# Optimization experiments

Hardware: AMD Instinct MI355X
Metric: run time of the kernel (lower is better)

The kernel has to match this reference:

```python
import jax, jax.numpy as jnp
import numpy as np

C = 1.0
SQC = C ** 0.5
EPS = 1e-15

def _artanh(x):
    return jnp.arctanh(jnp.clip(x, -1 + 1e-5, 1 - 1e-5))

def _norm(x):
    return jnp.sqrt(jnp.maximum(jnp.sum(x * x, -1, keepdims=True), EPS))

def expmap0(u):
    un = _norm(u)
    return jnp.tanh(SQC * un) * u / (SQC * un)

def logmap0(x):
    xn = _norm(x)
    return _artanh(SQC * xn) * x / (SQC * xn)

def project(x):
    maxnorm = (1.0 - 1e-3) / SQC
    xn = _norm(x)
    return jnp.where(xn > maxnorm, x / xn * maxnorm, x)

def mobius_add(x, y):
    x2 = jnp.sum(x * x, -1, keepdims=True)
    y2 = jnp.sum(y * y, -1, keepdims=True)
    xy = jnp.sum(x * y, -1, keepdims=True)
    num = (1 + 2 * C * xy + C * y2) * x + (1 - C * x2) * y
    den = 1 + 2 * C * xy + C * C * x2 * y2
    return num / jnp.maximum(den, EPS)

def mobius_matvec(M, x):
    xn = _norm(x)
    Mx = x @ M.T
    Mxn = _norm(Mx)
    res = jnp.tanh(Mxn / xn * _artanh(SQC * xn)) * Mx / (Mxn * SQC)
    return jnp.where(Mxn <= 1e-7, jnp.zeros_like(res), res)

def mobius_pointwise_mul(w, x):
    xn = _norm(x)
    wx = w * x
    wxn = _norm(wx)
    res = jnp.tanh(wxn / xn * _artanh(SQC * xn)) * wx / (wxn * SQC)
    return jnp.where(wxn <= 1e-7, jnp.zeros_like(res), res)

def mobius_scalar_mul(r, x):
    # r: [B,1] scalars, x: [P] point -> [B,P]
    xn = _norm(x)
    return jnp.tanh(r * _artanh(SQC * xn)) * x / (xn * SQC)

def poincare_dist(x, y):
    return 2.0 / SQC * _artanh(SQC * _norm(mobius_add(-x, y)))

def dist2plane(x, p, a):
    # x: [B,P], p,a: [K,P] -> [B,K]
    diff = mobius_add(-p[None, :, :], x[:, None, :])  # [B,K,P]
    diff2 = jnp.sum(diff * diff, -1)
    sc_da = jnp.sum(diff * a[None, :, :], -1)
    a_norm = jnp.sqrt(jnp.maximum(jnp.sum(a * a, -1), EPS))  # [K]
    num = 2 * SQC * sc_da
    den = jnp.maximum((1 - C * diff2) * a_norm[None, :], EPS)
    return jnp.arcsinh(num / den) / SQC

def one_rnn_transform(W, h, U, x, b):
    Wh = mobius_matvec(W, h)
    Ux = mobius_matvec(U, x)
    return mobius_add(mobius_add(Wh, Ux), b)

def mobius_gru(x_seq, w_ih, w_hh, b, h0):
    # x_seq: [S,B,E]; w_ih: [3,H,E]; w_hh: [3,H,H]; b: [3,H]
    W_ir, W_ih_, W_iz = w_ih[0], w_ih[1], w_ih[2]
    W_hr, W_hh_, W_hz = w_hh[0], w_hh[1], w_hh[2]
    b_r, b_h, b_z = b[0], b[1], b[2]

    def cell(h, x):
        z = jax.nn.sigmoid(logmap0(one_rnn_transform(W_hz, h, W_iz, x, b_z)))
        r = jax.nn.sigmoid(logmap0(one_rnn_transform(W_hr, h, W_ir, x, b_r)))
        rh = mobius_pointwise_mul(r, h)
        h_tilde = one_rnn_transform(W_hh_, rh, W_ih_, x, b_h)
        delta = mobius_add(-h, h_tilde)
        h_new = mobius_add(h, mobius_pointwise_mul(z, delta))
        return h_new, None

    h_final, _ = jax.lax.scan(cell, h0, x_seq)
    return h_final

def mobius_linear(x, W, b):
    return project(mobius_add(mobius_matvec(W, x), b))


def setup_inputs() -> dict:
    key = jax.random.key(0)
    ks = jax.random.split(key, 20)
    V, E, H, P, K, B, S = 32000, 256, 512, 256, 2, 512, 100
    inp = {
        "embedding": jax.random.normal(ks[0], (V, E), jnp.float32) * 0.1,
        "w_ih_src": jax.random.normal(ks[1], (3, H, E), jnp.float32) * 0.05,
        "w_hh_src": jax.random.normal(ks[2], (3, H, H), jnp.float32) * 0.05,
        "b_src": jax.random.normal(ks[3], (3, H), jnp.float32) * 0.01,
        "w_ih_tgt": jax.random.normal(ks[4], (3, H, E), jnp.float32) * 0.05,
        "w_hh_tgt": jax.random.normal(ks[5], (3, H, H), jnp.float32) * 0.05,
        "b_tgt": jax.random.normal(ks[6], (3, H), jnp.float32) * 0.01,
        "wp_src": jax.random.normal(ks[7], (P, H), jnp.float32) * 0.05,
        "bp_src": jax.random.normal(ks[8], (P,), jnp.float32) * 0.01,
        "wp_tgt": jax.random.normal(ks[9], (P, H), jnp.float32) * 0.05,
        "bp_tgt": jax.random.normal(ks[10], (P,), jnp.float32) * 0.01,
        "dist_bias": jax.random.normal(ks[11], (P,), jnp.float32) * 0.01,
        "plane_p": jax.random.normal(ks[12], (K, P), jnp.float32) * 0.01,
        "plane_a": jax.random.normal(ks[13], (K, P), jnp.float32) * 0.1,
        "source_tokens": jax.random.randint(ks[14], (B, S), 0, V, jnp.int32),
        "target_tokens": jax.random.randint(ks[15], (B, S), 0, V, jnp.int32),
        "alignment": jax.random.randint(ks[16], (B,), 0, B, jnp.int32),
    }
    return inp


def reference(embedding, w_ih_src, w_hh_src, b_src, w_ih_tgt, w_hh_tgt, b_tgt,
              wp_src, bp_src, wp_tgt, bp_tgt, dist_bias, plane_p, plane_a,
              source_tokens, target_tokens, alignment):
    B, S = source_tokens.shape
    H = w_hh_src.shape[-1]
    # euclidean embeddings lifted to the Poincare ball (embedding_type='eucl', hyp cell)
    src = expmap0(embedding[source_tokens]).transpose(1, 0, 2)  # [S,B,E]
    tgt = expmap0(embedding[target_tokens]).transpose(1, 0, 2)
    h0 = jnp.zeros((B, H), src.dtype)
    h_src = mobius_gru(src, w_ih_src, w_hh_src, b_src, h0)
    h_tgt = mobius_gru(tgt, w_ih_tgt, w_hh_tgt, b_tgt, h0)
    h_tgt = h_tgt[alignment]
    src_proj = mobius_linear(h_src, wp_src, bp_src)
    tgt_proj = mobius_linear(h_tgt, wp_tgt, bp_tgt)
    projected = mobius_add(src_proj, tgt_proj)
    d2 = poincare_dist(h_src, h_tgt) ** 2  # [B,1]
    bias = mobius_scalar_mul(d2, dist_bias)  # [B,P]
    projected = mobius_add(projected, bias)
    logits = dist2plane(projected, plane_p, plane_a)  # [B,K]
    return logits
```

## Files before the change

kernel.cpp:

```cpp
#include <hip/hip_runtime.h>
#include <hip/hip_bf16.h>

#define EPSF 1e-15f

__device__ __forceinline__ float artanh_c(float x) {
  x = fminf(fmaxf(x, -1.f + 1e-5f), 1.f - 1e-5f);
  return 0.5f * log1pf(2.f * x / (1.f - x));
}
__device__ __forceinline__ float sigmoidf(float x) {
  return 1.f / (1.f + expf(-x));
}

template<int N>
__device__ __forceinline__ void block_reduce(float* v) {
  __shared__ float s[4][N];
  __syncthreads();
  const int lane = threadIdx.x & 63;
  const int wv = threadIdx.x >> 6;
#pragma unroll
  for (int n = 0; n < N; n++) {
    float x = v[n];
#pragma unroll
    for (int o = 32; o > 0; o >>= 1) x += __shfl_down(x, o);
    if (lane == 0) s[wv][n] = x;
  }
  __syncthreads();
#pragma unroll
  for (int n = 0; n < N; n++) v[n] = s[0][n] + s[1][n] + s[2][n] + s[3][n];
}

__global__ __launch_bounds__(256) void k_tok(
    const float* __restrict__ emb, const int* __restrict__ src_t,
    const int* __restrict__ tgt_t, float4* __restrict__ tokf)
{
  const int item = blockIdx.x * 4 + (threadIdx.x >> 6);
  const int lane = threadIdx.x & 63;
  const int g = item / 51200;
  const int rem = item - g * 51200;
  const int b = rem / 100, s = rem - b * 100;
  const int tok = (g ? tgt_t : src_t)[b * 100 + s];
  const float4 v = ((const float4*)(emb + (size_t)tok * 256))[lane];
  float ss = v.x*v.x + v.y*v.y + v.z*v.z + v.w*v.w;
#pragma unroll
  for (int o = 32; o > 0; o >>= 1) ss += __shfl_xor(ss, o);
  if (lane == 0) {
    const float un = sqrtf(fmaxf(ss, EPSF));
    const float fac = tanhf(un) / un;
    const float xn = sqrtf(fmaxf(fac * fac * ss, EPSF));
    const float axn = artanh_c(xn);
    tokf[item] = make_float4(fac, xn, axn, un);
  }
}

__global__ __launch_bounds__(256) void kx0(
    const float* __restrict__ emb, const int* __restrict__ src_t,
    const int* __restrict__ tgt_t, const float4* __restrict__ tokf,
    float* __restrict__ xb)
{
  const int row = blockIdx.x;
  const int t = threadIdx.x;
  const int g = row >> 9, b = row & 511;
  const int tok = (g ? tgt_t : src_t)[b * 100];
  const float fac = tokf[(g * 512 + b) * 100].x;
  xb[(size_t)row * 256 + t] = fac * emb[(size_t)tok * 256 + t];
}

__global__ __launch_bounds__(256) void gemm_k(
    int mode,
    const float* __restrict__ hbuf, const float* __restrict__ xbuf,
    const float* __restrict__ rhbuf,
    const float* __restrict__ w_ih_src, const float* __restrict__ w_hh_src,
    const float* __restrict__ w_ih_tgt, const float* __restrict__ w_hh_tgt,
    const float* __restrict__ wp_src, const float* __restrict__ wp_tgt,
    const int* __restrict__ alignment,
    float* __restrict__ out)
{
  const int rt = blockIdx.x, ct = blockIdx.y;
  const int rowBase = rt * 64;
  const int tid = threadIdx.x;
  int kdim, ldo, colBase;
  const float* W;
  const float* Abase;
  int gather = 0;
  if (mode == 0) {
    const int chunk = ct >> 3;
    colBase = ct * 64; ldo = 2560;
    const int g = rowBase >> 9;
    const float* wih = g ? w_ih_tgt : w_ih_src;
    const float* whh = g ? w_hh_tgt : w_hh_src;
    if (chunk == 0)      { W = whh + 2 * 512 * 512; Abase = hbuf; kdim = 512; }
    else if (chunk == 1) { W = whh;                 Abase = hbuf; kdim = 512; }
    else {
      kdim = 256; Abase = xbuf;
      W = (chunk == 2) ? (wih + 2 * 512 * 256) : ((chunk == 3) ? wih : (wih + 512 * 256));
    }
    W += (size_t)((ct & 7) * 64) * kdim;
  } else if (mode == 1) {
    const int g = rowBase >> 9;
    W = (g ? w_hh_tgt : w_hh_src) + 512 * 512 + (size_t)(ct * 64) * 512;
    Abase = rhbuf; kdim = 512; ldo = 512; colBase = ct * 64;
  } else {
    const int chunk = ct >> 2;
    colBase = ct * 64; ldo = 512; kdim = 512;
    W = (chunk ? wp_tgt : wp_src) + (size_t)((ct & 3) * 64) * 512;
    Abase = hbuf;
    gather = chunk;
  }
  const int ar = tid >> 2, ak = (tid & 3) * 4;
  int arow = rowBase + ar;
  if (mode == 2 && gather) arow = 512 + alignment[arow];
  const float* Arow = Abase + (size_t)arow * kdim;
  const float* Wrow = W + (size_t)(tid >> 2) * kdim + (tid & 3) * 4;

  __shared__ __align__(16) float As[16][68];
  __shared__ __align__(16) float Bs[16][68];
  float acc[4][4] = {{0.f}};
  const int ty = tid >> 4, tx = tid & 15;

  for (int k0 = 0; k0 < kdim; k0 += 16) {
    const float4 av = *(const float4*)(Arow + k0 + ak);
    const float4 bv = *(const float4*)(Wrow + k0);
    const int bj = tid >> 2;
    As[ak + 0][ar] = av.x; As[ak + 1][ar] = av.y; As[ak + 2][ar] = av.z; As[ak + 3][ar] = av.w;
    Bs[ak + 0][bj] = bv.x; Bs[ak + 1][bj] = bv.y; Bs[ak + 2][bj] = bv.z; Bs[ak + 3][bj] = bv.w;
    __syncthreads();
#pragma unroll
    for (int kk = 0; kk < 16; kk++) {
      const float4 a4 = *(const float4*)(&As[kk][ty * 4]);
      const float4 b4 = *(const float4*)(&Bs[kk][tx * 4]);
      acc[0][0] += a4.x * b4.x; acc[0][1] += a4.x * b4.y; acc[0][2] += a4.x * b4.z; acc[0][3] += a4.x * b4.w;
      acc[1][0] += a4.y * b4.x; acc[1][1] += a4.y * b4.y; acc[1][2] += a4.y * b4.z; acc[1][3] += a4.y * b4.w;
      acc[2][0] += a4.z * b4.x; acc[2][1] += a4.z * b4.y; acc[2][2] += a4.z * b4.z; acc[2][3] += a4.z * b4.w;
      acc[3][0] += a4.w * b4.x; acc[3][1] += a4.w * b4.y; acc[3][2] += a4.w * b4.z; acc[3][3] += a4.w * b4.w;
    }
    __syncthreads();
  }
#pragma unroll
  for (int r = 0; r < 4; r++) {
    float4 o; o.x = acc[r][0]; o.y = acc[r][1]; o.z = acc[r][2]; o.w = acc[r][3];
    *(float4*)(out + (size_t)(rowBase + ty * 4 + r) * ldo + colBase + tx * 4) = o;
  }
}

__global__ __launch_bounds__(256) void k2_gates(
    const float* __restrict__ g1, const float* __restrict__ hb,
    const float* __restrict__ b_src, const float* __restrict__ b_tgt,
    const float4* __restrict__ tokf,
    float* __restrict__ zb, float* __restrict__ rhb,
    float* __restrict__ uhxb, float* __restrict__ rn, int s)
{
  const int row = blockIdx.x;
  const int g = row >> 9, b = row & 511;
  const int t = threadIdx.x;
  const float* bb = g ? b_tgt : b_src;
  const float4 tf = tokf[(g * 512 + b) * 100 + s];
  const float xn_x = tf.y, axn_x = tf.z;
  const float* grow = g1 + (size_t)row * 2560;
  const float* hrow = hb + (size_t)row * 512;

  float h[2], whz[2], whr[2], uxz[2], uxr[2], uxh[2], bz[2], br[2];
  float r6[6] = {0, 0, 0, 0, 0, 0};
#pragma unroll
  for (int e = 0; e < 2; e++) {
    const int j = t + e * 256;
    h[e] = hrow[j];
    whz[e] = grow[j];        whr[e] = grow[512 + j];
    uxz[e] = grow[1024 + j]; uxr[e] = grow[1536 + j];
    uxh[e] = grow[2048 + j];
    bz[e] = bb[1024 + j];    br[e] = bb[j];
    r6[0] += h[e] * h[e];     r6[1] += whz[e] * whz[e]; r6[2] += whr[e] * whr[e];
    r6[3] += uxz[e] * uxz[e]; r6[4] += uxr[e] * uxr[e]; r6[5] += uxh[e] * uxh[e];
  }
  block_reduce<6>(r6);
  const float sh2 = r6[0];
  const float xn_h = sqrtf(fmaxf(sh2, EPSF)), axn_h = artanh_c(xn_h);

  const float mz = sqrtf(fmaxf(r6[1], EPSF)); const float tz = tanhf(mz / xn_h * axn_h);
  const float sz = (mz <= 1e-7f) ? 0.f : tz / mz; const float x2z = (mz <= 1e-7f) ? 0.f : tz * tz;
  const float mr = sqrtf(fmaxf(r6[2], EPSF)); const float tr = tanhf(mr / xn_h * axn_h);
  const float sr = (mr <= 1e-7f) ? 0.f : tr / mr; const float x2r = (mr <= 1e-7f) ? 0.f : tr * tr;
  const float muz = sqrtf(fmaxf(r6[3], EPSF)); const float tuz = tanhf(muz / xn_x * axn_x);
  const float suz = (muz <= 1e-7f) ? 0.f : tuz / muz; const float y2z = (muz <= 1e-7f) ? 0.f : tuz * tuz;
  const float mur = sqrtf(fmaxf(r6[4], EPSF)); const float tur = tanhf(mur / xn_x * axn_x);
  const float sur = (mur <= 1e-7f) ? 0.f : tur / mur; const float y2r = (mur <= 1e-7f) ? 0.f : tur * tur;
  const float muh = sqrtf(fmaxf(r6[5], EPSF)); const float tuh = tanhf(muh / xn_x * axn_x);
  const float suh = (muh <= 1e-7f) ? 0.f : tuh / muh; const float y2u = (muh <= 1e-7f) ? 0.f : tuh * tuh;

  float Wz[2], Uz[2], Wr[2], Ur[2];
  float dd[2] = {0, 0};
#pragma unroll
  for (int e = 0; e < 2; e++) {
    Wz[e] = sz * whz[e]; Uz[e] = suz * uxz[e];
    Wr[e] = sr * whr[e]; Ur[e] = sur * uxr[e];
    dd[0] += Wz[e] * Uz[e]; dd[1] += Wr[e] * Ur[e];
  }
  block_reduce<2>(dd);
  float t1z[2], t1r[2];
  {
    const float xy = dd[0];
    const float iv = 1.f / fmaxf(1.f + 2.f * xy + x2z * y2z, EPSF);
    const float c1 = 1.f + 2.f * xy + y2z, c2 = 1.f - x2z;
#pragma unroll
    for (int e = 0; e < 2; e++) t1z[e] = (c1 * Wz[e] + c2 * Uz[e]) * iv;
  }
  {
    const float xy = dd[1];
    const float iv = 1.f / fmaxf(1.f + 2.f * xy + x2r * y2r, EPSF);
    const float c1 = 1.f + 2.f * xy + y2r, c2 = 1.f - x2r;
#pragma unroll
    for (int e = 0; e < 2; e++) t1r[e] = (c1 * Wr[e] + c2 * Ur[e]) * iv;
  }
  float r6b[6] = {0, 0, 0, 0, 0, 0};
#pragma unroll
  for (int e = 0; e < 2; e++) {
    r6b[0] += t1z[e] * t1z[e]; r6b[1] += t1z[e] * bz[e]; r6b[2] += bz[e] * bz[e];
    r6b[3] += t1r[e] * t1r[e]; r6b[4] += t1r[e] * br[e]; r6b[5] += br[e] * br[e];
  }
  block_reduce<6>(r6b);
  float t2z[2], t2r[2];
  {
    const float x2 = r6b[0], xy = r6b[1], y2 = r6b[2];
    const float iv = 1.f / fmaxf(1.f + 2.f * xy + x2 * y2, EPSF);
    const float c1 = 1.f + 2.f * xy + y2, c2 = 1.f - x2;
#pragma unroll
    for (int e = 0; e < 2; e++) t2z[e] = (c1 * t1z[e] + c2 * bz[e]) * iv;
  }
  {
    const float x2 = r6b[3], xy = r6b[4], y2 = r6b[5];
    const float iv = 1.f / fmaxf(1.f + 2.f * xy + x2 * y2, EPSF);
    const float c1 = 1.f + 2.f * xy + y2, c2 = 1.f - x2;
#pragma unroll
    for (int e = 0; e < 2; e++) t2r[e] = (c1 * t1r[e] + c2 * br[e]) * iv;
  }
  float nn[2] = {0, 0};
#pragma unroll
  for (int e = 0; e < 2; e++) { nn[0] += t2z[e] * t2z[e]; nn[1] += t2r[e] * t2r[e]; }
  block_reduce<2>(nn);
  const float nz = sqrtf(fmaxf(nn[0], EPSF)); const float fz = artanh_c(nz) / nz;
  const float nr = sqrtf(fmaxf(nn[1], EPSF)); const float fr = artanh_c(nr) / nr;
  float zz[2], wx[2];
  float rw[1] = {0};
#pragma unroll
  for (int e = 0; e < 2; e++) {
    zz[e] = sigmoidf(fz * t2z[e]);
    const float rr = sigmoidf(fr * t2r[e]);
    wx[e] = rr * h[e];
    rw[0] += wx[e] * wx[e];
  }
  block_reduce<1>(rw);
  const float wxn = sqrtf(fmaxf(rw[0], EPSF));
  const float trh = tanhf(wxn / xn_h * axn_h);
  const float srh = (wxn <= 1e-7f) ? 0.f : trh / wxn;
  const float xn_rh = (wxn <= 1e-7f) ? sqrtf(EPSF) : fmaxf(trh, sqrtf(EPSF));
  const float axn_rh = artanh_c(xn_rh);
#pragma unroll
  for (int e = 0; e < 2; e++) {
    const int j = t + e * 256;
    zb[(size_t)row * 512 + j] = zz[e];
    rhb[(size_t)row * 512 + j] = srh * wx[e];
    uhxb[(size_t)row * 512 + j] = suh * uxh[e];
  }
  if (t == 0) {
    float* r8 = rn + row * 8;
    r8[0] = xn_h; r8[1] = axn_h; r8[2] = xn_rh; r8[3] = axn_rh; r8[4] = y2u; r8[5] = sh2;
  }
}

__global__ __launch_bounds__(256) void k4_update(
    const float* __restrict__ htm, const float* __restrict__ uhxb,
    const float* __restrict__ zb, float* __restrict__ hb,
    const float* __restrict__ b_src, const float* __restrict__ b_tgt,
    const float* __restrict__ rn, const float4* __restrict__ tokf,
    const int* __restrict__ src_t, const int* __restrict__ tgt_t,
    const float* __restrict__ emb, float* __restrict__ xb, int s)
{
  const int row = blockIdx.x;
  const int g = row >> 9, b = row & 511;
  const int t = threadIdx.x;
  const float* bb = g ? b_tgt : b_src;
  const float* r8 = rn + row * 8;
  const float xn_rh = r8[2], axn_rh = r8[3], y2u = r8[4], sh2 = r8[5];

  float mt_[2], ux[2], z[2], h[2], bh[2];
  float rA[2] = {0, 0};
#pragma unroll
  for (int e = 0; e < 2; e++) {
    const int j = t + e * 256;
    mt_[e] = htm[(size_t)row * 512 + j];
    ux[e] = uhxb[(size_t)row * 512 + j];
    z[e] = zb[(size_t)row * 512 + j];
    h[e] = hb[(size_t)row * 512 + j];
    bh[e] = bb[512 + j];
    rA[0] += mt_[e] * mt_[e];
    rA[1] += mt_[e] * ux[e];
  }
  block_reduce<2>(rA);
  const float m = sqrtf(fmaxf(rA[0], EPSF));
  const float tt = tanhf(m / xn_rh * axn_rh);
  const float st = (m <= 1e-7f) ? 0.f : tt / m;
  const float x2 = (m <= 1e-7f) ? 0.f : tt * tt;
  float t1[2];
  {
    const float xy = st * rA[1];
    const float iv = 1.f / fmaxf(1.f + 2.f * xy + x2 * y2u, EPSF);
    const float c1 = 1.f + 2.f * xy + y2u, c2 = 1.f - x2;
#pragma unroll
    for (int e = 0; e < 2; e++) t1[e] = (c1 * (st * mt_[e]) + c2 * ux[e]) * iv;
  }
  float rB[3] = {0, 0, 0};
#pragma unroll
  for (int e = 0; e < 2; e++) {
    rB[0] += t1[e] * t1[e]; rB[1] += t1[e] * bh[e]; rB[2] += bh[e] * bh[e];
  }
  block_reduce<3>(rB);
  float ht[2];
  {
    const float x2b = rB[0], xy = rB[1], y2 = rB[2];
    const float iv = 1.f / fmaxf(1.f + 2.f * xy + x2b * y2, EPSF);
    const float c1 = 1.f + 2.f * xy + y2, c2 = 1.f - x2b;
#pragma unroll
    for (int e = 0; e < 2; e++) ht[e] = (c1 * t1[e] + c2 * bh[e]) * iv;
  }
  float rC[2] = {0, 0};
#pragma unroll
  for (int e = 0; e < 2; e++) { rC[0] += ht[e] * ht[e]; rC[1] += h[e] * ht[e]; }
  block_reduce<2>(rC);
  float delta[2];
  {
    const float y2 = rC[0], xy = -rC[1];
    const float iv = 1.f / fmaxf(1.f + 2.f * xy + sh2 * y2, EPSF);
    const float c1 = 1.f + 2.f * xy + y2, c2 = 1.f - sh2;
#pragma unroll
    for (int e = 0; e < 2; e++) delta[e] = (c1 * (-h[e]) + c2 * ht[e]) * iv;
  }
  float rD[3] = {0, 0, 0};
#pragma unroll
  for (int e = 0; e < 2; e++) {
    const float w = z[e] * delta[e];
    rD[0] += delta[e] * delta[e];
    rD[1] += w * w;
    rD[2] += h[e] * w;
  }
  block_reduce<3>(rD);
  const float dn = sqrtf(fmaxf(rD[0], EPSF));
  const float axnd = artanh_c(dn);
  const float wxn = sqrtf(fmaxf(rD[1], EPSF));
  const float tzd = tanhf(wxn / dn * axnd);
  const float szd = (wxn <= 1e-7f) ? 0.f : tzd / wxn;
  const float y2zd = (wxn <= 1e-7f) ? 0.f : tzd * tzd;
  {
    const float xy = szd * rD[2];
    const float iv = 1.f / fmaxf(1.f + 2.f * xy + sh2 * y2zd, EPSF);
    const float c1 = 1.f + 2.f * xy + y2zd, c2 = 1.f - sh2;
#pragma unroll
    for (int e = 0; e < 2; e++) {
      const int j = t + e * 256;
      hb[(size_t)row * 512 + j] = (c1 * h[e] + c2 * (szd * z[e] * delta[e])) * iv;
    }
  }
  if (s + 1 < 100) {
    const int tok = (g ? tgt_t : src_t)[b * 100 + s + 1];
    const float fac = tokf[(g * 512 + b) * 100 + s + 1].x;
    xb[(size_t)row * 256 + t] = fac * emb[(size_t)tok * 256 + t];
  }
}

__global__ __launch_bounds__(256) void k_head(
    const float* __restrict__ hb, const float* __restrict__ mxb,
    const float* __restrict__ bp_src, const float* __restrict__ bp_tgt,
    const float* __restrict__ dist_bias, const float* __restrict__ plane_p,
    const float* __restrict__ plane_a, const int* __restrict__ alignment,
    float* __restrict__ outp)
{
  const int b = blockIdx.x;
  const int t = threadIdx.x;
  const int arow = 512 + alignment[b];
  float hs[2], htg[2];
  hs[0] = hb[(size_t)b * 512 + t];      hs[1] = hb[(size_t)b * 512 + 256 + t];
  htg[0] = hb[(size_t)arow * 512 + t];  htg[1] = hb[(size_t)arow * 512 + 256 + t];
  const float mxs = mxb[(size_t)b * 512 + t];
  const float mxt = mxb[(size_t)b * 512 + 256 + t];
  const float bps = bp_src[t], bpt = bp_tgt[t], db = dist_bias[t];
  const float pp0 = plane_p[t], pp1 = plane_p[256 + t];
  const float pa0 = plane_a[t], pa1 = plane_a[256 + t];

  float rA[5] = {0, 0, 0, 0, 0};
#pragma unroll
  for (int e = 0; e < 2; e++) {
    rA[0] += hs[e] * hs[e]; rA[1] += htg[e] * htg[e]; rA[2] += hs[e] * htg[e];
  }
  rA[3] = mxs * mxs; rA[4] = mxt * mxt;
  block_reduce<5>(rA);
  const float shs = rA[0], sht = rA[1], dot_st = rA[2];
  const float xns = sqrtf(fmaxf(shs, EPSF)), axns = artanh_c(xns);
  const float xnt = sqrtf(fmaxf(sht, EPSF)), axnt = artanh_c(xnt);
  const float ms = sqrtf(fmaxf(rA[3], EPSF)); const float ts = tanhf(ms / xns * axns);
  const float ss = (ms <= 1e-7f) ? 0.f : ts / ms; const float x2s = (ms <= 1e-7f) ? 0.f : ts * ts;
  const float mt = sqrtf(fmaxf(rA[4], EPSF)); const float tt = tanhf(mt / xnt * axnt);
  const float st = (mt <= 1e-7f) ? 0.f : tt / mt; const float x2t = (mt <= 1e-7f) ? 0.f : tt * tt;
  const float vs = ss * mxs, vt = st * mxt;

  float rB[5] = {bps * bps, vs * bps, bpt * bpt, vt * bpt, db * db};
  block_reduce<5>(rB);
  float ps, pt;
  {
    const float y2 = rB[0], xy = rB[1];
    const float iv = 1.f / fmaxf(1.f + 2.f * xy + x2s * y2, EPSF);
    ps = ((1.f + 2.f * xy + y2) * vs + (1.f - x2s) * bps) * iv;
  }
  {
    const float y2 = rB[2], xy = rB[3];
    const float iv = 1.f / fmaxf(1.f + 2.f * xy + x2t * y2, EPSF);
    pt = ((1.f + 2.f * xy + y2) * vt + (1.f - x2t) * bpt) * iv;
  }
  float rC[2] = {ps * ps, pt * pt};
  block_reduce<2>(rC);
  {
    const float n = sqrtf(fmaxf(rC[0], EPSF));
    if (n > 0.999f) ps *= 0.999f / n;
  }
  {
    const float n = sqrtf(fmaxf(rC[1], EPSF));
    if (n > 0.999f) pt *= 0.999f / n;
  }
  float df[2];
  {
    const float xy = -dot_st;
    const float iv = 1.f / fmaxf(1.f + 2.f * xy + shs * sht, EPSF);
    const float c1 = 1.f + 2.f * xy + sht, c2 = 1.f - shs;
#pragma unroll
    for (int e = 0; e < 2; e++) df[e] = (c1 * (-hs[e]) + c2 * htg[e]) * iv;
  }
  float rD[4] = {ps * ps, pt * pt, ps * pt, df[0] * df[0] + df[1] * df[1]};
  block_reduce<4>(rD);
  float pr;
  {
    const float x2 = rD[0], y2 = rD[1], xy = rD[2];
    const float iv = 1.f / fmaxf(1.f + 2.f * xy + x2 * y2, EPSF);
    pr = ((1.f + 2.f * xy + y2) * ps + (1.f - x2) * pt) * iv;
  }
  const float dn = sqrtf(fmaxf(rD[3], EPSF));
  const float dist = 2.f * artanh_c(dn);
  const float d2v = dist * dist;
  const float dbn = sqrtf(fmaxf(rB[4], EPSF));
  const float biasv = tanhf(d2v * artanh_c(dbn)) * db / dbn;

  float rE[3] = {pr * pr, biasv * biasv, pr * biasv};
  block_reduce<3>(rE);
  float pr2;
  {
    const float x2 = rE[0], y2 = rE[1], xy = rE[2];
    const float iv = 1.f / fmaxf(1.f + 2.f * xy + x2 * y2, EPSF);
    pr2 = ((1.f + 2.f * xy + y2) * pr + (1.f - x2) * biasv) * iv;
  }
  float rF[5] = {pp0 * pp0, pp0 * pr2, pp1 * pp1, pp1 * pr2, pr2 * pr2};
  block_reduce<5>(rF);
  float d0, d1;
  {
    const float x2 = rF[0], xy = -rF[1], y2 = rF[4];
    const float iv = 1.f / fmaxf(1.f + 2.f * xy + x2 * y2, EPSF);
    d0 = ((1.f + 2.f * xy + y2) * (-pp0) + (1.f - x2) * pr2) * iv;
  }
  {
    const float x2 = rF[2], xy = -rF[3], y2 = rF[4];
    const float iv = 1.f / fmaxf(1.f + 2.f * xy + x2 * y2, EPSF);
    d1 = ((1.f + 2.f * xy + y2) * (-pp1) + (1.f - x2) * pr2) * iv;
  }
  float rG[6] = {d0 * d0, d0 * pa0, pa0 * pa0, d1 * d1, d1 * pa1, pa1 * pa1};
  block_reduce<6>(rG);
  if (t == 0) {
    const float an0 = sqrtf(fmaxf(rG[2], EPSF));
    const float an1 = sqrtf(fmaxf(rG[5], EPSF));
    const float l0 = asinhf(2.f * rG[1] / fmaxf((1.f - rG[0]) * an0, EPSF));
    const float l1 = asinhf(2.f * rG[4] / fmaxf((1.f - rG[3]) * an1, EPSF));
    outp[b * 2 + 0] = l0;
    outp[b * 2 + 1] = l1;
  }
}

extern "C" void kernel_launch(void* const* d_in, const int* in_sizes, int n_in,
                              void* d_out, int out_size, void* d_ws, size_t ws_size,
                              hipStream_t stream) {
  const float* emb       = (const float*)d_in[0];
  const float* w_ih_src  = (const float*)d_in[1];
  const float* w_hh_src  = (const float*)d_in[2];
  const float* b_src     = (const float*)d_in[3];
  const float* w_ih_tgt  = (const float*)d_in[4];
  const float* w_hh_tgt  = (const float*)d_in[5];
  const float* b_tgt     = (const float*)d_in[6];
  const float* wp_src    = (const float*)d_in[7];
  const float* bp_src    = (const float*)d_in[8];
  const float* wp_tgt    = (const float*)d_in[9];
  const float* bp_tgt    = (const float*)d_in[10];
  const float* dist_bias = (const float*)d_in[11];
  const float* plane_p   = (const float*)d_in[12];
  const float* plane_a   = (const float*)d_in[13];
  const int* src_t       = (const int*)d_in[14];
  const int* tgt_t       = (const int*)d_in[15];
  const int* alignment   = (const int*)d_in[16];
  float* outp            = (float*)d_out;

  float* ws = (float*)d_ws;
  float* hbuf = ws + 0;
  float* xbuf = ws + 524288;
  float* g1   = ws + 786432;
  float* zb   = ws + 3407872;
  float* rhb  = ws + 3932160;
  float* uhxb = ws + 4456448;
  float* htm  = ws + 4980736;
  float* rn   = ws + 5505024;
  float4* tokf = (float4*)(ws + 5513216);
  float* mxb  = ws + 5922816;

  hipMemsetAsync(hbuf, 0, 1024 * 512 * sizeof(float), stream);
  k_tok<<<25600, 256, 0, stream>>>(emb, src_t, tgt_t, tokf);
  kx0<<<1024, 256, 0, stream>>>(emb, src_t, tgt_t, tokf, xbuf);
  for (int s = 0; s < 100; s++) {
    gemm_k<<<dim3(16, 40), 256, 0, stream>>>(0, hbuf, xbuf, rhb,
        w_ih_src, w_hh_src, w_ih_tgt, w_hh_tgt, wp_src, wp_tgt, alignment, g1);
    k2_gates<<<1024, 256, 0, stream>>>(g1, hbuf, b_src, b_tgt, tokf, zb, rhb, uhxb, rn, s);
    gemm_k<<<dim3(16, 8), 256, 0, stream>>>(1, hbuf, xbuf, rhb,
        w_ih_src, w_hh_src, w_ih_tgt, w_hh_tgt, wp_src, wp_tgt, alignment, htm);
    k4_update<<<1024, 256, 0, stream>>>(htm, uhxb, zb, hbuf, b_src, b_tgt, rn, tokf,
        src_t, tgt_t, emb, xbuf, s);
  }
  gemm_k<<<dim3(8, 8), 256, 0, stream>>>(2, hbuf, xbuf, rhb,
      w_ih_src, w_hh_src, w_ih_tgt, w_hh_tgt, wp_src, wp_tgt, alignment, mxb);
  k_head<<<512, 256, 0, stream>>>(hbuf, mxb, bp_src, bp_tgt, dist_bias,
      plane_p, plane_a, alignment, outp);
}
```

Before: 8.037 ms.

## Replace per-step kernel launches with cooperative persistent kernel using split-bf16 MFMA

Replaces the 400 per-timestep launches (two FP32 SIMT GEMMs plus gate and update kernels) with one cooperative persistent kernel that uses grid syncs between phases. The GEMMs now run on MFMA bf16 instructions with a hi/lo split (three products) to approximate FP32 accuracy, using weights pre-split by a new conversion kernel. Row reductions move from block-level shared-memory reductions to wave-level shuffles. This removes launch overhead and scalar FMA cost, but relies on grid-wide barriers and accepts slightly lower precision from dropping the lo*lo term.

```diff
diff --git a/kernel.cpp b/kernel.cpp
--- a/kernel.cpp
+++ b/kernel.cpp
@@ -1,32 +1,71 @@
 #include <hip/hip_runtime.h>
 #include <hip/hip_bf16.h>
+#include <hip/hip_cooperative_groups.h>
+
+namespace cg = cooperative_groups;
 
 #define EPSF 1e-15f
+
+typedef __hip_bfloat16 bf16;
+typedef __attribute__((ext_vector_type(8))) short short8;
+typedef __attribute__((ext_vector_type(4))) float f32x4;
+
+#define F4E(v,i) ((i)==0?(v).x:((i)==1?(v).y:((i)==2?(v).z:(v).w)))
+#define U4E(v,i) ((i)==0?(v).x:((i)==1?(v).y:((i)==2?(v).z:(v).w)))
 
 __device__ __forceinline__ float artanh_c(float x) {
   x = fminf(fmaxf(x, -1.f + 1e-5f), 1.f - 1e-5f);
   return 0.5f * log1pf(2.f * x / (1.f - x));
 }
-__device__ __forceinline__ float sigmoidf(float x) {
-  return 1.f / (1.f + expf(-x));
-}
-
-template<int N>
-__device__ __forceinline__ void block_reduce(float* v) {
-  __shared__ float s[4][N];
-  __syncthreads();
-  const int lane = threadIdx.x & 63;
-  const int wv = threadIdx.x >> 6;
-#pragma unroll
-  for (int n = 0; n < N; n++) {
-    float x = v[n];
-#pragma unroll
-    for (int o = 32; o > 0; o >>= 1) x += __shfl_down(x, o);
-    if (lane == 0) s[wv][n] = x;
-  }
-  __syncthreads();
-#pragma unroll
-  for (int n = 0; n < N; n++) v[n] = s[0][n] + s[1][n] + s[2][n] + s[3][n];
+__device__ __forceinline__ float sigmoidf(float x) { return 1.f / (1.f + expf(-x)); }
+__device__ __forceinline__ float wave_sum(float x) {
+#pragma unroll
+  for (int o = 32; o > 0; o >>= 1) x += __shfl_xor(x, o);
+  return x;
+}
+__device__ __forceinline__ float bu2f(ushort u) { return __uint_as_float(((unsigned)u) << 16); }
+__device__ __forceinline__ ushort f2bu(float v) {
+  bf16 t = __float2bfloat16(v);
+  union { bf16 b; ushort u; } c; c.b = t; return c.u;
+}
+__device__ __forceinline__ void split2(float v, ushort& h, ushort& l) {
+  h = f2bu(v); l = f2bu(v - bu2f(h));
+}
+
+__global__ __launch_bounds__(256) void k_wconv(
+    const float* __restrict__ w_ih_src, const float* __restrict__ w_hh_src,
+    const float* __restrict__ w_ih_tgt, const float* __restrict__ w_hh_tgt,
+    const float* __restrict__ wp_src, const float* __restrict__ wp_tgt,
+    bf16* __restrict__ W0h, bf16* __restrict__ W0l,
+    bf16* __restrict__ W1h, bf16* __restrict__ W1l,
+    bf16* __restrict__ W2h, bf16* __restrict__ W2l)
+{
+  const int idx = blockIdx.x * 256 + threadIdx.x;
+  float v; bf16 *ph, *pl; int oi;
+  if (idx < 1835008) {
+    const int g = idx / 917504, r = idx % 917504;
+    const float* wih = g ? w_ih_tgt : w_ih_src;
+    const float* whh = g ? w_hh_tgt : w_hh_src;
+    if (r < 262144)      v = whh[524288 + r];
+    else if (r < 524288) v = whh[r - 262144];
+    else if (r < 655360) v = wih[262144 + (r - 524288)];
+    else if (r < 786432) v = wih[r - 655360];
+    else                 v = wih[131072 + (r - 786432)];
+    ph = W0h; pl = W0l; oi = idx;
+  } else if (idx < 2359296) {
+    const int j = idx - 1835008;
+    const int g = j >> 18, r = j & 262143;
+    v = (g ? w_hh_tgt : w_hh_src)[262144 + r];
+    ph = W1h; pl = W1l; oi = j;
+  } else {
+    const int p = idx - 2359296;
+    if (p >= 262144) return;
+    const int g = p >> 17, r = p & 131071;
+    v = (g ? wp_tgt : wp_src)[r];
+    ph = W2h; pl = W2l; oi = p;
+  }
+  ushort hh, ll; split2(v, hh, ll);
+  ((ushort*)ph)[oi] = hh; ((ushort*)pl)[oi] = ll;
 }
 
 __global__ __launch_bounds__(256) void k_tok(
@@ -47,434 +86,579 @@
     const float un = sqrtf(fmaxf(ss, EPSF));
     const float fac = tanhf(un) / un;
     const float xn = sqrtf(fmaxf(fac * fac * ss, EPSF));
-    const float axn = artanh_c(xn);
-    tokf[item] = make_float4(fac, xn, axn, un);
+    tokf[item] = make_float4(fac, xn, artanh_c(xn), un);
   }
 }
 
 __global__ __launch_bounds__(256) void kx0(
     const float* __restrict__ emb, const int* __restrict__ src_t,
     const int* __restrict__ tgt_t, const float4* __restrict__ tokf,
-    float* __restrict__ xb)
+    bf16* __restrict__ Xh, bf16* __restrict__ Xl)
 {
   const int row = blockIdx.x;
   const int t = threadIdx.x;
   const int g = row >> 9, b = row & 511;
   const int tok = (g ? tgt_t : src_t)[b * 100];
   const float fac = tokf[(g * 512 + b) * 100].x;
-  xb[(size_t)row * 256 + t] = fac * emb[(size_t)tok * 256 + t];
-}
-
-__global__ __launch_bounds__(256) void gemm_k(
-    int mode,
-    const float* __restrict__ hbuf, const float* __restrict__ xbuf,
-    const float* __restrict__ rhbuf,
-    const float* __restrict__ w_ih_src, const float* __restrict__ w_hh_src,
-    const float* __restrict__ w_ih_tgt, const float* __restrict__ w_hh_tgt,
-    const float* __restrict__ wp_src, const float* __restrict__ wp_tgt,
-    const int* __restrict__ alignment,
-    float* __restrict__ out)
+  ushort hh, ll; split2(fac * emb[(size_t)tok * 256 + t], hh, ll);
+  ((ushort*)Xh)[(size_t)row * 256 + t] = hh;
+  ((ushort*)Xl)[(size_t)row * 256 + t] = ll;
+}
+
+__device__ __forceinline__ void mma_32x32(
+    const bf16* __restrict__ Ah, const bf16* __restrict__ Al,
+    size_t a0, size_t a1,
+    const bf16* __restrict__ Wh, const bf16* __restrict__ Wl,
+    size_t b0, size_t b1, int K,
+    float* __restrict__ outB, int ldo, int kg)
 {
-  const int rt = blockIdx.x, ct = blockIdx.y;
-  const int rowBase = rt * 64;
+  f32x4 acc00 = {0,0,0,0}, acc01 = {0,0,0,0}, acc10 = {0,0,0,0}, acc11 = {0,0,0,0};
+#pragma unroll 2
+  for (int k0 = 0; k0 < K; k0 += 32) {
+    const short8 a0h = *(const short8*)(Ah + a0 + k0);
+    const short8 a0l = *(const short8*)(Al + a0 + k0);
+    const short8 a1h = *(const short8*)(Ah + a1 + k0);
+    const short8 a1l = *(const short8*)(Al + a1 + k0);
+    const short8 b0h = *(const short8*)(Wh + b0 + k0);
+    const short8 b0l = *(const short8*)(Wl + b0 + k0);
+    const short8 b1h = *(const short8*)(Wh + b1 + k0);
+    const short8 b1l = *(const short8*)(Wl + b1 + k0);
+    acc00 = __builtin_amdgcn_mfma_f32_16x16x32_bf16(a0h, b0h, acc00, 0, 0, 0);
+    acc01 = __builtin_amdgcn_mfma_f32_16x16x32_bf16(a0h, b1h, acc01, 0, 0, 0);
+    acc10 = __builtin_amdgcn_mfma_f32_16x16x32_bf16(a1h, b0h, acc10, 0, 0, 0);
+    acc11 = __builtin_amdgcn_mfma_f32_16x16x32_bf16(a1h, b1h, acc11, 0, 0, 0);
+    acc00 = __builtin_amdgcn_mfma_f32_16x16x32_bf16(a0h, b0l, acc00, 0, 0, 0);
+    acc01 = __builtin_amdgcn_mfma_f32_16x16x32_bf16(a0h, b1l, acc01, 0, 0, 0);
+    acc10 = __builtin_amdgcn_mfma_f32_16x16x32_bf16(a1h, b0l, acc10, 0, 0, 0);
+    acc11 = __builtin_amdgcn_mfma_f32_16x16x32_bf16(a1h, b1l, acc11, 0, 0, 0);
+    acc00 = __builtin_amdgcn_mfma_f32_16x16x32_bf16(a0l, b0h, acc00, 0, 0, 0);
+    acc01 = __builtin_amdgcn_mfma_f32_16x16x32_bf16(a0l, b1h, acc01, 0, 0, 0);
+    acc10 = __builtin_amdgcn_mfma_f32_16x16x32_bf16(a1l, b0h, acc10, 0, 0, 0);
+    acc11 = __builtin_amdgcn_mfma_f32_16x16x32_bf16(a1l, b1h, acc11, 0, 0, 0);
+  }
+#pragma unroll
+  for (int r = 0; r < 4; r++) {
+    outB[(size_t)(kg*4 + r) * ldo]            = acc00[r];
+    outB[(size_t)(kg*4 + r) * ldo + 16]       = acc01[r];
+    outB[(size_t)(16 + kg*4 + r) * ldo]       = acc10[r];
+    outB[(size_t)(16 + kg*4 + r) * ldo + 16]  = acc11[r];
+  }
+}
+
+__device__ __forceinline__ void mma_32x16(
+    const bf16* __restrict__ Ah, const bf16* __restrict__ Al,
+    size_t a0, size_t a1,
+    const bf16* __restrict__ Wh, const bf16* __restrict__ Wl,
+    size_t b0, int K,
+    float* __restrict__ outB, int ldo, int kg)
+{
+  f32x4 acc0 = {0,0,0,0}, acc1 = {0,0,0,0};
+#pragma unroll 2
+  for (int k0 = 0; k0 < K; k0 += 32) {
+    const short8 a0h = *(const short8*)(Ah + a0 + k0);
+    const short8 a0l = *(const short8*)(Al + a0 + k0);
+    const short8 a1h = *(const short8*)(Ah + a1 + k0);
+    const short8 a1l = *(const short8*)(Al + a1 + k0);
+    const short8 bh  = *(const short8*)(Wh + b0 + k0);
+    const short8 bl  = *(const short8*)(Wl + b0 + k0);
+    acc0 = __builtin_amdgcn_mfma_f32_16x16x32_bf16(a0h, bh, acc0, 0, 0, 0);
+    acc1 = __builtin_amdgcn_mfma_f32_16x16x32_bf16(a1h, bh, acc1, 0, 0, 0);
+    acc0 = __builtin_amdgcn_mfma_f32_16x16x32_bf16(a0h, bl, acc0, 0, 0, 0);
+    acc1 = __builtin_amdgcn_mfma_f32_16x16x32_bf16(a1h, bl, acc1, 0, 0, 0);
+    acc0 = __builtin_amdgcn_mfma_f32_16x16x32_bf16(a0l, bh, acc0, 0, 0, 0);
+    acc1 = __builtin_amdgcn_mfma_f32_16x16x32_bf16(a1l, bh, acc1, 0, 0, 0);
+  }
+#pragma unroll
+  for (int r = 0; r < 4; r++) {
+    outB[(size_t)(kg*4 + r) * ldo]      = acc0[r];
+    outB[(size_t)(16 + kg*4 + r) * ldo] = acc1[r];
+  }
+}
+
+__device__ __forceinline__ void phaseA_tile(
+    int tr, int tc, int wr, int wc, int fr, int kg,
+    const bf16* Hh, const bf16* Hl, const bf16* Xh, const bf16* Xl,
+    const bf16* W0h, const bf16* W0l, float* g1)
+{
+  const int g = tr >> 9;
+  int K; const bf16 *Ah, *Al; size_t Woff;
+  if (tc < 1024) {
+    K = 512; Ah = Hh; Al = Hl;
+    Woff = (size_t)g*917504 + (size_t)(tc>>9)*262144 + (size_t)(tc & 511)*512;
+  } else {
+    K = 256; Ah = Xh; Al = Xl;
+    const int lc = tc - 1024;
+    Woff = (size_t)g*917504 + 524288 + (size_t)(lc>>9)*131072 + (size_t)(lc & 511)*256;
+  }
+  const int r0 = tr + wr*32;
+  const size_t a0 = (size_t)(r0 + fr)*K + kg*8, a1 = a0 + (size_t)16*K;
+  const size_t b0 = (size_t)(wc*32 + fr)*K + kg*8, b1 = b0 + (size_t)16*K;
+  float* outB = g1 + (size_t)r0*2560 + (tc + wc*32 + fr);
+  mma_32x32(Ah, Al, a0, a1, W0h + Woff, W0l + Woff, b0, b1, K, outB, 2560, kg);
+}
+
+struct CoopArgs {
+  const float *emb; const int *src_t, *tgt_t;
+  const float *b_src, *b_tgt, *bp_src, *bp_tgt, *dist_bias, *plane_p, *plane_a;
+  const int *alignment;
+  float *g1, *htm, *hbuf, *mxb;
+  const float4 *tokf;
+  bf16 *Hh, *Hl, *Xh, *Xl, *Rh, *Rl;
+  const bf16 *W0h, *W0l, *W1h, *W1l, *W2h, *W2l;
+  float *outp;
+};
+
+__global__ __launch_bounds__(512, 2) void k_coop(CoopArgs A)
+{
+  cg::grid_group grid = cg::this_grid();
+  const int bid = blockIdx.x;
   const int tid = threadIdx.x;
-  int kdim, ldo, colBase;
-  const float* W;
-  const float* Abase;
-  int gather = 0;
-  if (mode == 0) {
-    const int chunk = ct >> 3;
-    colBase = ct * 64; ldo = 2560;
-    const int g = rowBase >> 9;
-    const float* wih = g ? w_ih_tgt : w_ih_src;
-    const float* whh = g ? w_hh_tgt : w_hh_src;
-    if (chunk == 0)      { W = whh + 2 * 512 * 512; Abase = hbuf; kdim = 512; }
-    else if (chunk == 1) { W = whh;                 Abase = hbuf; kdim = 512; }
-    else {
-      kdim = 256; Abase = xbuf;
-      W = (chunk == 2) ? (wih + 2 * 512 * 256) : ((chunk == 3) ? wih : (wih + 512 * 256));
-    }
-    W += (size_t)((ct & 7) * 64) * kdim;
-  } else if (mode == 1) {
-    const int g = rowBase >> 9;
-    W = (g ? w_hh_tgt : w_hh_src) + 512 * 512 + (size_t)(ct * 64) * 512;
-    Abase = rhbuf; kdim = 512; ldo = 512; colBase = ct * 64;
+  const int w = tid >> 6, lane = tid & 63;
+  const int fr = lane & 15, kg = lane >> 4;
+  const int wrA = w >> 1, wcA = w & 1;
+  const int wrC = w >> 2, wcC = w & 3;
+
+  int An, t0r = 0, t0c = 0, t1r = 0, t1c = 0;
+  if (bid < 128) {
+    An = 1; t0r = (bid >> 4) * 128; t0c = (bid & 15) * 64;
   } else {
-    const int chunk = ct >> 2;
-    colBase = ct * 64; ldo = 512; kdim = 512;
-    W = (chunk ? wp_tgt : wp_src) + (size_t)((ct & 3) * 64) * 512;
-    Abase = hbuf;
-    gather = chunk;
-  }
-  const int ar = tid >> 2, ak = (tid & 3) * 4;
-  int arow = rowBase + ar;
-  if (mode == 2 && gather) arow = 512 + alignment[arow];
-  const float* Arow = Abase + (size_t)arow * kdim;
-  const float* Wrow = W + (size_t)(tid >> 2) * kdim + (tid & 3) * 4;
-
-  __shared__ __align__(16) float As[16][68];
-  __shared__ __align__(16) float Bs[16][68];
-  float acc[4][4] = {{0.f}};
-  const int ty = tid >> 4, tx = tid & 15;
-
-  for (int k0 = 0; k0 < kdim; k0 += 16) {
-    const float4 av = *(const float4*)(Arow + k0 + ak);
-    const float4 bv = *(const float4*)(Wrow + k0);
-    const int bj = tid >> 2;
-    As[ak + 0][ar] = av.x; As[ak + 1][ar] = av.y; As[ak + 2][ar] = av.z; As[ak + 3][ar] = av.w;
-    Bs[ak + 0][bj] = bv.x; Bs[ak + 1][bj] = bv.y; Bs[ak + 2][bj] = bv.z; Bs[ak + 3][bj] = bv.w;
-    __syncthreads();
-#pragma unroll
-    for (int kk = 0; kk < 16; kk++) {
-      const float4 a4 = *(const float4*)(&As[kk][ty * 4]);
-      const float4 b4 = *(const float4*)(&Bs[kk][tx * 4]);
-      acc[0][0] += a4.x * b4.x; acc[0][1] += a4.x * b4.y; acc[0][2] += a4.x * b4.z; acc[0][3] += a4.x * b4.w;
-      acc[1][0] += a4.y * b4.x; acc[1][1] += a4.y * b4.y; acc[1][2] += a4.y * b4.z; acc[1][3] += a4.y * b4.w;
-      acc[2][0] += a4.z * b4.x; acc[2][1] += a4.z * b4.y; acc[2][2] += a4.z * b4.z; acc[2][3] += a4.z * b4.w;
-      acc[3][0] += a4.w * b4.x; acc[3][1] += a4.w * b4.y; acc[3][2] += a4.w * b4.z; acc[3][3] += a4.w * b4.w;
-    }
-    __syncthreads();
-  }
-#pragma unroll
-  for (int r = 0; r < 4; r++) {
-    float4 o; o.x = acc[r][0]; o.y = acc[r][1]; o.z = acc[r][2]; o.w = acc[r][3];
-    *(float4*)(out + (size_t)(rowBase + ty * 4 + r) * ldo + colBase + tx * 4) = o;
-  }
-}
-
-__global__ __launch_bounds__(256) void k2_gates(
-    const float* __restrict__ g1, const float* __restrict__ hb,
-    const float* __restrict__ b_src, const float* __restrict__ b_tgt,
-    const float4* __restrict__ tokf,
-    float* __restrict__ zb, float* __restrict__ rhb,
-    float* __restrict__ uhxb, float* __restrict__ rn, int s)
-{
-  const int row = blockIdx.x;
-  const int g = row >> 9, b = row & 511;
-  const int t = threadIdx.x;
-  const float* bb = g ? b_tgt : b_src;
-  const float4 tf = tokf[(g * 512 + b) * 100 + s];
-  const float xn_x = tf.y, axn_x = tf.z;
-  const float* grow = g1 + (size_t)row * 2560;
-  const float* hrow = hb + (size_t)row * 512;
-
-  float h[2], whz[2], whr[2], uxz[2], uxr[2], uxh[2], bz[2], br[2];
-  float r6[6] = {0, 0, 0, 0, 0, 0};
-#pragma unroll
-  for (int e = 0; e < 2; e++) {
-    const int j = t + e * 256;
-    h[e] = hrow[j];
-    whz[e] = grow[j];        whr[e] = grow[512 + j];
-    uxz[e] = grow[1024 + j]; uxr[e] = grow[1536 + j];
-    uxh[e] = grow[2048 + j];
-    bz[e] = bb[1024 + j];    br[e] = bb[j];
-    r6[0] += h[e] * h[e];     r6[1] += whz[e] * whz[e]; r6[2] += whr[e] * whr[e];
-    r6[3] += uxz[e] * uxz[e]; r6[4] += uxr[e] * uxr[e]; r6[5] += uxh[e] * uxh[e];
-  }
-  block_reduce<6>(r6);
-  const float sh2 = r6[0];
-  const float xn_h = sqrtf(fmaxf(sh2, EPSF)), axn_h = artanh_c(xn_h);
-
-  const float mz = sqrtf(fmaxf(r6[1], EPSF)); const float tz = tanhf(mz / xn_h * axn_h);
-  const float sz = (mz <= 1e-7f) ? 0.f : tz / mz; const float x2z = (mz <= 1e-7f) ? 0.f : tz * tz;
-  const float mr = sqrtf(fmaxf(r6[2], EPSF)); const float tr = tanhf(mr / xn_h * axn_h);
-  const float sr = (mr <= 1e-7f) ? 0.f : tr / mr; const float x2r = (mr <= 1e-7f) ? 0.f : tr * tr;
-  const float muz = sqrtf(fmaxf(r6[3], EPSF)); const float tuz = tanhf(muz / xn_x * axn_x);
-  const float suz = (muz <= 1e-7f) ? 0.f : tuz / muz; const float y2z = (muz <= 1e-7f) ? 0.f : tuz * tuz;
-  const float mur = sqrtf(fmaxf(r6[4], EPSF)); const float tur = tanhf(mur / xn_x * axn_x);
-  const float sur = (mur <= 1e-7f) ? 0.f : tur / mur; const float y2r = (mur <= 1e-7f) ? 0.f : tur * tur;
-  const float muh = sqrtf(fmaxf(r6[5], EPSF)); const float tuh = tanhf(muh / xn_x * axn_x);
-  const float suh = (muh <= 1e-7f) ? 0.f : tuh / muh; const float y2u = (muh <= 1e-7f) ? 0.f : tuh * tuh;
-
-  float Wz[2], Uz[2], Wr[2], Ur[2];
-  float dd[2] = {0, 0};
-#pragma unroll
-  for (int e = 0; e < 2; e++) {
-    Wz[e] = sz * whz[e]; Uz[e] = suz * uxz[e];
-    Wr[e] = sr * whr[e]; Ur[e] = sur * uxr[e];
-    dd[0] += Wz[e] * Uz[e]; dd[1] += Wr[e] * Ur[e];
-  }
-  block_reduce<2>(dd);
-  float t1z[2], t1r[2];
-  {
-    const float xy = dd[0];
-    const float iv = 1.f / fmaxf(1.f + 2.f * xy + x2z * y2z, EPSF);
-    const float c1 = 1.f + 2.f * xy + y2z, c2 = 1.f - x2z;
-#pragma unroll
-    for (int e = 0; e < 2; e++) t1z[e] = (c1 * Wz[e] + c2 * Uz[e]) * iv;
-  }
-  {
-    const float xy = dd[1];
-    const float iv = 1.f / fmaxf(1.f + 2.f * xy + x2r * y2r, EPSF);
-    const float c1 = 1.f + 2.f * xy + y2r, c2 = 1.f - x2r;
-#pragma unroll
-    for (int e = 0; e < 2; e++) t1r[e] = (c1 * Wr[e] + c2 * Ur[e]) * iv;
-  }
-  float r6b[6] = {0, 0, 0, 0, 0, 0};
-#pragma unroll
-  for (int e = 0; e < 2; e++) {
-    r6b[0] += t1z[e] * t1z[e]; r6b[1] += t1z[e] * bz[e]; r6b[2] += bz[e] * bz[e];
-    r6b[3] += t1r[e] * t1r[e]; r6b[4] += t1r[e] * br[e]; r6b[5] += br[e] * br[e];
-  }
-  block_reduce<6>(r6b);
-  float t2z[2], t2r[2];
-  {
-    const float x2 = r6b[0], xy = r6b[1], y2 = r6b[2];
-    const float iv = 1.f / fmaxf(1.f + 2.f * xy + x2 * y2, EPSF);
-    const float c1 = 1.f + 2.f * xy + y2, c2 = 1.f - x2;
-#pragma unroll
-    for (int e = 0; e < 2; e++) t2z[e] = (c1 * t1z[e] + c2 * bz[e]) * iv;
-  }
-  {
-    const float x2 = r6b[3], xy = r6b[4], y2 = r6b[5];
-    const float iv = 1.f / fmaxf(1.f + 2.f * xy + x2 * y2, EPSF);
-    const float c1 = 1.f + 2.f * xy + y2, c2 = 1.f - x2;
-#pragma unroll
-    for (int e = 0; e < 2; e++) t2r[e] = (c1 * t1r[e] + c2 * br[e]) * iv;
-  }
-  float nn[2] = {0, 0};
-#pragma unroll
-  for (int e = 0; e < 2; e++) { nn[0] += t2z[e] * t2z[e]; nn[1] += t2r[e] * t2r[e]; }
-  block_reduce<2>(nn);
-  const float nz = sqrtf(fmaxf(nn[0], EPSF)); const float fz = artanh_c(nz) / nz;
-  const float nr = sqrtf(fmaxf(nn[1], EPSF)); const float fr = artanh_c(nr) / nr;
-  float zz[2], wx[2];
-  float rw[1] = {0};
-#pragma unroll
-  for (int e = 0; e < 2; e++) {
-    zz[e] = sigmoidf(fz * t2z[e]);
-    const float rr = sigmoidf(fr * t2r[e]);
-    wx[e] = rr * h[e];
-    rw[0] += wx[e] * wx[e];
-  }
-  block_reduce<1>(rw);
-  const float wxn = sqrtf(fmaxf(rw[0], EPSF));
-  const float trh = tanhf(wxn / xn_h * axn_h);
-  const float srh = (wxn <= 1e-7f) ? 0.f : trh / wxn;
-  const float xn_rh = (wxn <= 1e-7f) ? sqrtf(EPSF) : fmaxf(trh, sqrtf(EPSF));
-  const float axn_rh = artanh_c(xn_rh);
-#pragma unroll
-  for (int e = 0; e < 2; e++) {
-    const int j = t + e * 256;
-    zb[(size_t)row * 512 + j] = zz[e];
-    rhb[(size_t)row * 512 + j] = srh * wx[e];
-    uhxb[(size_t)row * 512 + j] = suh * uxh[e];
-  }
-  if (t == 0) {
-    float* r8 = rn + row * 8;
-    r8[0] = xn_h; r8[1] = axn_h; r8[2] = xn_rh; r8[3] = axn_rh; r8[4] = y2u; r8[5] = sh2;
-  }
-}
-
-__global__ __launch_bounds__(256) void k4_update(
-    const float* __restrict__ htm, const float* __restrict__ uhxb,
-    const float* __restrict__ zb, float* __restrict__ hb,
-    const float* __restrict__ b_src, const float* __restrict__ b_tgt,
-    const float* __restrict__ rn, const float4* __restrict__ tokf,
-    const int* __restrict__ src_t, const int* __restrict__ tgt_t,
-    const float* __restrict__ emb, float* __restrict__ xb, int s)
-{
-  const int row = blockIdx.x;
-  const int g = row >> 9, b = row & 511;
-  const int t = threadIdx.x;
-  const float* bb = g ? b_tgt : b_src;
-  const float* r8 = rn + row * 8;
-  const float xn_rh = r8[2], axn_rh = r8[3], y2u = r8[4], sh2 = r8[5];
-
-  float mt_[2], ux[2], z[2], h[2], bh[2];
-  float rA[2] = {0, 0};
-#pragma unroll
-  for (int e = 0; e < 2; e++) {
-    const int j = t + e * 256;
-    mt_[e] = htm[(size_t)row * 512 + j];
-    ux[e] = uhxb[(size_t)row * 512 + j];
-    z[e] = zb[(size_t)row * 512 + j];
-    h[e] = hb[(size_t)row * 512 + j];
-    bh[e] = bb[512 + j];
-    rA[0] += mt_[e] * mt_[e];
-    rA[1] += mt_[e] * ux[e];
-  }
-  block_reduce<2>(rA);
-  const float m = sqrtf(fmaxf(rA[0], EPSF));
-  const float tt = tanhf(m / xn_rh * axn_rh);
-  const float st = (m <= 1e-7f) ? 0.f : tt / m;
-  const float x2 = (m <= 1e-7f) ? 0.f : tt * tt;
-  float t1[2];
-  {
-    const float xy = st * rA[1];
-    const float iv = 1.f / fmaxf(1.f + 2.f * xy + x2 * y2u, EPSF);
-    const float c1 = 1.f + 2.f * xy + y2u, c2 = 1.f - x2;
-#pragma unroll
-    for (int e = 0; e < 2; e++) t1[e] = (c1 * (st * mt_[e]) + c2 * ux[e]) * iv;
-  }
-  float rB[3] = {0, 0, 0};
-#pragma unroll
-  for (int e = 0; e < 2; e++) {
-    rB[0] += t1[e] * t1[e]; rB[1] += t1[e] * bh[e]; rB[2] += bh[e] * bh[e];
-  }
-  block_reduce<3>(rB);
-  float ht[2];
-  {
-    const float x2b = rB[0], xy = rB[1], y2 = rB[2];
-    const float iv = 1.f / fmaxf(1.f + 2.f * xy + x2b * y2, EPSF);
-    const float c1 = 1.f + 2.f * xy + y2, c2 = 1.f - x2b;
-#pragma unroll
-    for (int e = 0; e < 2; e++) ht[e] = (c1 * t1[e] + c2 * bh[e]) * iv;
-  }
-  float rC[2] = {0, 0};
-#pragma unroll
-  for (int e = 0; e < 2; e++) { rC[0] += ht[e] * ht[e]; rC[1] += h[e] * ht[e]; }
-  block_reduce<2>(rC);
-  float delta[2];
-  {
-    const float y2 = rC[0], xy = -rC[1];
-    const float iv = 1.f / fmaxf(1.f + 2.f * xy + sh2 * y2, EPSF);
-    const float c1 = 1.f + 2.f * xy + y2, c2 = 1.f - sh2;
-#pragma unroll
-    for (int e = 0; e < 2; e++) delta[e] = (c1 * (-h[e]) + c2 * ht[e]) * iv;
-  }
-  float rD[3] = {0, 0, 0};
-#pragma unroll
-  for (int e = 0; e < 2; e++) {
-    const float w = z[e] * delta[e];
-    rD[0] += delta[e] * delta[e];
-    rD[1] += w * w;
-    rD[2] += h[e] * w;
-  }
-  block_reduce<3>(rD);
-  const float dn = sqrtf(fmaxf(rD[0], EPSF));
-  const float axnd = artanh_c(dn);
-  const float wxn = sqrtf(fmaxf(rD[1], EPSF));
-  const float tzd = tanhf(wxn / dn * axnd);
-  const float szd = (wxn <= 1e-7f) ? 0.f : tzd / wxn;
-  const float y2zd = (wxn <= 1e-7f) ? 0.f : tzd * tzd;
-  {
-    const float xy = szd * rD[2];
-    const float iv = 1.f / fmaxf(1.f + 2.f * xy + sh2 * y2zd, EPSF);
-    const float c1 = 1.f + 2.f * xy + y2zd, c2 = 1.f - sh2;
-#pragma unroll
-    for (int e = 0; e < 2; e++) {
-      const int j = t + e * 256;
-      hb[(size_t)row * 512 + j] = (c1 * h[e] + c2 * (szd * z[e] * delta[e])) * iv;
-    }
-  }
-  if (s + 1 < 100) {
-    const int tok = (g ? tgt_t : src_t)[b * 100 + s + 1];
-    const float fac = tokf[(g * 512 + b) * 100 + s + 1].x;
-    xb[(size_t)row * 256 + t] = fac * emb[(size_t)tok * 256 + t];
-  }
-}
-
-__global__ __launch_bounds__(256) void k_head(
-    const float* __restrict__ hb, const float* __restrict__ mxb,
-    const float* __restrict__ bp_src, const float* __restrict__ bp_tgt,
-    const float* __restrict__ dist_bias, const float* __restrict__ plane_p,
-    const float* __restrict__ plane_a, const int* __restrict__ alignment,
-    float* __restrict__ outp)
-{
-  const int b = blockIdx.x;
-  const int t = threadIdx.x;
-  const int arow = 512 + alignment[b];
-  float hs[2], htg[2];
-  hs[0] = hb[(size_t)b * 512 + t];      hs[1] = hb[(size_t)b * 512 + 256 + t];
-  htg[0] = hb[(size_t)arow * 512 + t];  htg[1] = hb[(size_t)arow * 512 + 256 + t];
-  const float mxs = mxb[(size_t)b * 512 + t];
-  const float mxt = mxb[(size_t)b * 512 + 256 + t];
-  const float bps = bp_src[t], bpt = bp_tgt[t], db = dist_bias[t];
-  const float pp0 = plane_p[t], pp1 = plane_p[256 + t];
-  const float pa0 = plane_a[t], pa1 = plane_a[256 + t];
-
-  float rA[5] = {0, 0, 0, 0, 0};
-#pragma unroll
-  for (int e = 0; e < 2; e++) {
-    rA[0] += hs[e] * hs[e]; rA[1] += htg[e] * htg[e]; rA[2] += hs[e] * htg[e];
-  }
-  rA[3] = mxs * mxs; rA[4] = mxt * mxt;
-  block_reduce<5>(rA);
-  const float shs = rA[0], sht = rA[1], dot_st = rA[2];
-  const float xns = sqrtf(fmaxf(shs, EPSF)), axns = artanh_c(xns);
-  const float xnt = sqrtf(fmaxf(sht, EPSF)), axnt = artanh_c(xnt);
-  const float ms = sqrtf(fmaxf(rA[3], EPSF)); const float ts = tanhf(ms / xns * axns);
-  const float ss = (ms <= 1e-7f) ? 0.f : ts / ms; const float x2s = (ms <= 1e-7f) ? 0.f : ts * ts;
-  const float mt = sqrtf(fmaxf(rA[4], EPSF)); const float tt = tanhf(mt / xnt * axnt);
-  const float st = (mt <= 1e-7f) ? 0.f : tt / mt; const float x2t = (mt <= 1e-7f) ? 0.f : tt * tt;
-  const float vs = ss * mxs, vt = st * mxt;
-
-  float rB[5] = {bps * bps, vs * bps, bpt * bpt, vt * bpt, db * db};
-  block_reduce<5>(rB);
-  float ps, pt;
-  {
-    const float y2 = rB[0], xy = rB[1];
-    const float iv = 1.f / fmaxf(1.f + 2.f * xy + x2s * y2, EPSF);
-    ps = ((1.f + 2.f * xy + y2) * vs + (1.f - x2s) * bps) * iv;
-  }
-  {
-    const float y2 = rB[2], xy = rB[3];
-    const float iv = 1.f / fmaxf(1.f + 2.f * xy + x2t * y2, EPSF);
-    pt = ((1.f + 2.f * xy + y2) * vt + (1.f - x2t) * bpt) * iv;
-  }
-  float rC[2] = {ps * ps, pt * pt};
-  block_reduce<2>(rC);
-  {
-    const float n = sqrtf(fmaxf(rC[0], EPSF));
-    if (n > 0.999f) ps *= 0.999f / n;
-  }
-  {
-    const float n = sqrtf(fmaxf(rC[1], EPSF));
-    if (n > 0.999f) pt *= 0.999f / n;
-  }
-  float df[2];
-  {
-    const float xy = -dot_st;
-    const float iv = 1.f / fmaxf(1.f + 2.f * xy + shs * sht, EPSF);
-    const float c1 = 1.f + 2.f * xy + sht, c2 = 1.f - shs;
-#pragma unroll
-    for (int e = 0; e < 2; e++) df[e] = (c1 * (-hs[e]) + c2 * htg[e]) * iv;
-  }
-  float rD[4] = {ps * ps, pt * pt, ps * pt, df[0] * df[0] + df[1] * df[1]};
-  block_reduce<4>(rD);
-  float pr;
-  {
-    const float x2 = rD[0], y2 = rD[1], xy = rD[2];
-    const float iv = 1.f / fmaxf(1.f + 2.f * xy + x2 * y2, EPSF);
-    pr = ((1.f + 2.f * xy + y2) * ps + (1.f - x2) * pt) * iv;
-  }
-  const float dn = sqrtf(fmaxf(rD[3], EPSF));
-  const float dist = 2.f * artanh_c(dn);
-  const float d2v = dist * dist;
-  const float dbn = sqrtf(fmaxf(rB[4], EPSF));
-  const float biasv = tanhf(d2v * artanh_c(dbn)) * db / dbn;
-
-  float rE[3] = {pr * pr, biasv * biasv, pr * biasv};
-  block_reduce<3>(rE);
-  float pr2;
-  {
-    const float x2 = rE[0], y2 = rE[1], xy = rE[2];
-    const float iv = 1.f / fmaxf(1.f + 2.f * xy + x2 * y2, EPSF);
-    pr2 = ((1.f + 2.f * xy + y2) * pr + (1.f - x2) * biasv) * iv;
-  }
-  float rF[5] = {pp0 * pp0, pp0 * pr2, pp1 * pp1, pp1 * pr2, pr2 * pr2};
-  block_reduce<5>(rF);
-  float d0, d1;
-  {
-    const float x2 = rF[0], xy = -rF[1], y2 = rF[4];
-    const float iv = 1.f / fmaxf(1.f + 2.f * xy + x2 * y2, EPSF);
-    d0 = ((1.f + 2.f * xy + y2) * (-pp0) + (1.f - x2) * pr2) * iv;
-  }
-  {
-    const float x2 = rF[2], xy = -rF[3], y2 = rF[4];
-    const float iv = 1.f / fmaxf(1.f + 2.f * xy + x2 * y2, EPSF);
-    d1 = ((1.f + 2.f * xy + y2) * (-pp1) + (1.f - x2) * pr2) * iv;
-  }
-  float rG[6] = {d0 * d0, d0 * pa0, pa0 * pa0, d1 * d1, d1 * pa1, pa1 * pa1};
-  block_reduce<6>(rG);
-  if (t == 0) {
-    const float an0 = sqrtf(fmaxf(rG[2], EPSF));
-    const float an1 = sqrtf(fmaxf(rG[5], EPSF));
-    const float l0 = asinhf(2.f * rG[1] / fmaxf((1.f - rG[0]) * an0, EPSF));
-    const float l1 = asinhf(2.f * rG[4] / fmaxf((1.f - rG[3]) * an1, EPSF));
-    outp[b * 2 + 0] = l0;
-    outp[b * 2 + 1] = l1;
+    const int c8 = bid & 7, ii = (bid - 128) >> 3;
+    if (ii < 8) {
+      An = 2;
+      const int tp0 = 2*ii, tp1 = 2*ii + 1;
+      t0r = (tp0/3)*128; t0c = (16 + c8 + (tp0%3)*8) * 64;
+      t1r = (tp1/3)*128; t1c = (16 + c8 + (tp1%3)*8) * 64;
+    } else {
+      An = 1;
+      const int tp0 = 16 + (ii - 8);
+      t0r = (tp0/3)*128; t0c = (16 + c8 + (tp0%3)*8) * 64;
+    }
+  }
+
+  const int rowBD = bid * 4 + w;
+  float pz[8], puhx[8], ph[8];
+  float p_xnrh = 0.f, p_axnrh = 0.f, p_y2u = 0.f, p_sh2 = 0.f;
+
+  for (int s = 0; s < 100; s++) {
+    phaseA_tile(t0r, t0c, wrA, wcA, fr, kg, A.Hh, A.Hl, A.Xh, A.Xl, A.W0h, A.W0l, A.g1);
+    if (An == 2)
+      phaseA_tile(t1r, t1c, wrA, wcA, fr, kg, A.Hh, A.Hl, A.Xh, A.Xl, A.W0h, A.W0l, A.g1);
+    grid.sync();
+
+    if (w < 4) {
+      const int row = rowBD, g = row >> 9, b = row & 511;
+      const float* bb = g ? A.b_tgt : A.b_src;
+      const float4 tf = A.tokf[(g * 512 + b) * 100 + s];
+      const float xn_x = tf.y, axn_x = tf.z;
+      const float* grow = A.g1 + (size_t)row * 2560;
+      float h[8], whz[8], whr[8], uxz[8], uxr[8], uxh[8], bz[8], br[8];
+      float r60=0, r61=0, r62=0, r63=0, r64_=0, r65=0;
+#pragma unroll
+      for (int q = 0; q < 2; q++) {
+        const int j4 = lane + 64*q;
+        const ushort4 hhv = ((const ushort4*)(A.Hh + (size_t)row*512))[j4];
+        const ushort4 hlv = ((const ushort4*)(A.Hl + (size_t)row*512))[j4];
+        const float4 vz = ((const float4*)grow)[j4];
+        const float4 vr = ((const float4*)(grow + 512))[j4];
+        const float4 uz = ((const float4*)(grow + 1024))[j4];
+        const float4 ur = ((const float4*)(grow + 1536))[j4];
+        const float4 uh = ((const float4*)(grow + 2048))[j4];
+        const float4 vbz = ((const float4*)(bb + 1024))[j4];
+        const float4 vbr = ((const float4*)bb)[j4];
+#pragma unroll
+        for (int i = 0; i < 4; i++) {
+          const int e = q*4 + i;
+          h[e]  = bu2f(U4E(hhv,i)) + bu2f(U4E(hlv,i));
+          whz[e] = F4E(vz,i); whr[e] = F4E(vr,i);
+          uxz[e] = F4E(uz,i); uxr[e] = F4E(ur,i); uxh[e] = F4E(uh,i);
+          bz[e] = F4E(vbz,i); br[e] = F4E(vbr,i);
+          r60 += h[e]*h[e];     r61 += whz[e]*whz[e]; r62 += whr[e]*whr[e];
+          r63 += uxz[e]*uxz[e]; r64_ += uxr[e]*uxr[e]; r65 += uxh[e]*uxh[e];
+        }
+      }
+      r60 = wave_sum(r60); r61 = wave_sum(r61); r62 = wave_sum(r62);
+      r63 = wave_sum(r63); r64_ = wave_sum(r64_); r65 = wave_sum(r65);
+      const float sh2 = r60;
+      const float xn_h = sqrtf(fmaxf(sh2, EPSF)), axn_h = artanh_c(xn_h);
+      const float mz = sqrtf(fmaxf(r61, EPSF)); const float tz = tanhf(mz / xn_h * axn_h);
+      const float sz = (mz <= 1e-7f) ? 0.f : tz/mz; const float x2z = (mz <= 1e-7f) ? 0.f : tz*tz;
+      const float mr = sqrtf(fmaxf(r62, EPSF)); const float tr_ = tanhf(mr / xn_h * axn_h);
+      const float sr = (mr <= 1e-7f) ? 0.f : tr_/mr; const float x2r = (mr <= 1e-7f) ? 0.f : tr_*tr_;
+      const float muz = sqrtf(fmaxf(r63, EPSF)); const float tuz = tanhf(muz / xn_x * axn_x);
+      const float suz = (muz <= 1e-7f) ? 0.f : tuz/muz; const float y2z = (muz <= 1e-7f) ? 0.f : tuz*tuz;
+      const float mur = sqrtf(fmaxf(r64_, EPSF)); const float tur = tanhf(mur / xn_x * axn_x);
+      const float sur = (mur <= 1e-7f) ? 0.f : tur/mur; const float y2r = (mur <= 1e-7f) ? 0.f : tur*tur;
+      const float muh = sqrtf(fmaxf(r65, EPSF)); const float tuh = tanhf(muh / xn_x * axn_x);
+      const float suh = (muh <= 1e-7f) ? 0.f : tuh/muh; const float y2u = (muh <= 1e-7f) ? 0.f : tuh*tuh;
+
+      float Wz[8], Uz[8], Wr[8], Ur[8];
+      float dd0 = 0, dd1 = 0;
+#pragma unroll
+      for (int e = 0; e < 8; e++) {
+        Wz[e] = sz*whz[e]; Uz[e] = suz*uxz[e];
+        Wr[e] = sr*whr[e]; Ur[e] = sur*uxr[e];
+        dd0 += Wz[e]*Uz[e]; dd1 += Wr[e]*Ur[e];
+      }
+      dd0 = wave_sum(dd0); dd1 = wave_sum(dd1);
+      float t1z[8], t1r[8];
+      {
+        const float iv = 1.f / fmaxf(1.f + 2.f*dd0 + x2z*y2z, EPSF);
+        const float c1 = 1.f + 2.f*dd0 + y2z, c2 = 1.f - x2z;
+#pragma unroll
+        for (int e = 0; e < 8; e++) t1z[e] = (c1*Wz[e] + c2*Uz[e]) * iv;
+      }
+      {
+        const float iv = 1.f / fmaxf(1.f + 2.f*dd1 + x2r*y2r, EPSF);
+        const float c1 = 1.f + 2.f*dd1 + y2r, c2 = 1.f - x2r;
+#pragma unroll
+        for (int e = 0; e < 8; e++) t1r[e] = (c1*Wr[e] + c2*Ur[e]) * iv;
+      }
+      float e0=0, e1=0, e2=0, e3=0, e4=0, e5=0;
+#pragma unroll
+      for (int e = 0; e < 8; e++) {
+        e0 += t1z[e]*t1z[e]; e1 += t1z[e]*bz[e]; e2 += bz[e]*bz[e];
+        e3 += t1r[e]*t1r[e]; e4 += t1r[e]*br[e]; e5 += br[e]*br[e];
+      }
+      e0 = wave_sum(e0); e1 = wave_sum(e1); e2 = wave_sum(e2);
+      e3 = wave_sum(e3); e4 = wave_sum(e4); e5 = wave_sum(e5);
+      float t2z[8], t2r[8];
+      {
+        const float iv = 1.f / fmaxf(1.f + 2.f*e1 + e0*e2, EPSF);
+        const float c1 = 1.f + 2.f*e1 + e2, c2 = 1.f - e0;
+#pragma unroll
+        for (int e = 0; e < 8; e++) t2z[e] = (c1*t1z[e] + c2*bz[e]) * iv;
+      }
+      {
+        const float iv = 1.f / fmaxf(1.f + 2.f*e4 + e3*e5, EPSF);
+        const float c1 = 1.f + 2.f*e4 + e5, c2 = 1.f - e3;
+#pragma unroll
+        for (int e = 0; e < 8; e++) t2r[e] = (c1*t1r[e] + c2*br[e]) * iv;
+      }
+      float n0 = 0, n1 = 0;
+#pragma unroll
+      for (int e = 0; e < 8; e++) { n0 += t2z[e]*t2z[e]; n1 += t2r[e]*t2r[e]; }
+      n0 = wave_sum(n0); n1 = wave_sum(n1);
+      const float nz = sqrtf(fmaxf(n0, EPSF)); const float fz = artanh_c(nz) / nz;
+      const float nr = sqrtf(fmaxf(n1, EPSF)); const float frg = artanh_c(nr) / nr;
+      float zz[8], wx[8];
+      float rw = 0;
+#pragma unroll
+      for (int e = 0; e < 8; e++) {
+        zz[e] = sigmoidf(fz * t2z[e]);
+        const float rr = sigmoidf(frg * t2r[e]);
+        wx[e] = rr * h[e];
+        rw += wx[e]*wx[e];
+      }
+      rw = wave_sum(rw);
+      const float wxn = sqrtf(fmaxf(rw, EPSF));
+      const float trh = tanhf(wxn / xn_h * axn_h);
+      const float srh = (wxn <= 1e-7f) ? 0.f : trh / wxn;
+      const float xn_rh = (wxn <= 1e-7f) ? sqrtf(EPSF) : fmaxf(trh, sqrtf(EPSF));
+      const float axn_rh = artanh_c(xn_rh);
+#pragma unroll
+      for (int q = 0; q < 2; q++) {
+        ushort th[4], tl[4];
+#pragma unroll
+        for (int i = 0; i < 4; i++) split2(srh * wx[q*4+i], th[i], tl[i]);
+        ((ushort4*)(A.Rh + (size_t)row*512))[lane + 64*q] = make_ushort4(th[0],th[1],th[2],th[3]);
+        ((ushort4*)(A.Rl + (size_t)row*512))[lane + 64*q] = make_ushort4(tl[0],tl[1],tl[2],tl[3]);
+      }
+#pragma unroll
+      for (int e = 0; e < 8; e++) { pz[e] = zz[e]; puhx[e] = suh*uxh[e]; ph[e] = h[e]; }
+      p_xnrh = xn_rh; p_axnrh = axn_rh; p_y2u = y2u; p_sh2 = sh2;
+    }
+    grid.sync();
+
+    if (bid < 128) {
+      const int rows = (bid >> 3) * 64, cols = (bid & 7) * 64;
+      const int g = rows >> 9;
+      const size_t Woff = (size_t)g*262144 + (size_t)cols*512;
+      const int r0 = rows + wrC*32;
+      const size_t a0 = (size_t)(r0 + fr)*512 + kg*8, a1 = a0 + (size_t)16*512;
+      const size_t b0 = (size_t)(wcC*16 + fr)*512 + kg*8;
+      float* outB = A.htm + (size_t)r0*512 + (cols + wcC*16 + fr);
+      mma_32x16(A.Rh, A.Rl, a0, a1, A.W1h + Woff, A.W1l + Woff, b0, 512, outB, 512, kg);
+    }
+    grid.sync();
+
+    if (w < 4) {
+      const int row = rowBD, g = row >> 9, b = row & 511;
+      const float* bb = g ? A.b_tgt : A.b_src;
+      float mt_[8], bh[8];
+      float a0s = 0, a1s = 0;
+#pragma unroll
+      for (int q = 0; q < 2; q++) {
+        const int j4 = lane + 64*q;
+        const float4 vm = ((const float4*)(A.htm + (size_t)row*512))[j4];
+        const float4 vb = ((const float4*)(bb + 512))[j4];
+#pragma unroll
+        for (int i = 0; i < 4; i++) {
+          const int e = q*4 + i;
+          mt_[e] = F4E(vm,i); bh[e] = F4E(vb,i);
+          a0s += mt_[e]*mt_[e]; a1s += mt_[e]*puhx[e];
+        }
+      }
+      a0s = wave_sum(a0s); a1s = wave_sum(a1s);
+      const float m = sqrtf(fmaxf(a0s, EPSF));
+      const float tt = tanhf(m / p_xnrh * p_axnrh);
+      const float st = (m <= 1e-7f) ? 0.f : tt/m;
+      const float x2 = (m <= 1e-7f) ? 0.f : tt*tt;
+      float t1[8];
+      {
+        const float xy = st * a1s;
+        const float iv = 1.f / fmaxf(1.f + 2.f*xy + x2*p_y2u, EPSF);
+        const float c1 = 1.f + 2.f*xy + p_y2u, c2 = 1.f - x2;
+#pragma unroll
+        for (int e = 0; e < 8; e++) t1[e] = (c1*(st*mt_[e]) + c2*puhx[e]) * iv;
+      }
+      float b0s = 0, b1s = 0, b2s = 0;
+#pragma unroll
+      for (int e = 0; e < 8; e++) { b0s += t1[e]*t1[e]; b1s += t1[e]*bh[e]; b2s += bh[e]*bh[e]; }
+      b0s = wave_sum(b0s); b1s = wave_sum(b1s); b2s = wave_sum(b2s);
+      float ht[8];
+      {
+        const float iv = 1.f / fmaxf(1.f + 2.f*b1s + b0s*b2s, EPSF);
+        const float c1 = 1.f + 2.f*b1s + b2s, c2 = 1.f - b0s;
+#pragma unroll
+        for (int e = 0; e < 8; e++) ht[e] = (c1*t1[e] + c2*bh[e]) * iv;
+      }
+      float c0s = 0, c1s = 0;
+#pragma unroll
+      for (int e = 0; e < 8; e++) { c0s += ht[e]*ht[e]; c1s += ph[e]*ht[e]; }
+      c0s = wave_sum(c0s); c1s = wave_sum(c1s);
+      float delta[8];
+      {
+        const float xy = -c1s;
+        const float iv = 1.f / fmaxf(1.f + 2.f*xy + p_sh2*c0s, EPSF);
+        const float c1 = 1.f + 2.f*xy + c0s, c2 = 1.f - p_sh2;
+#pragma unroll
+        for (int e = 0; e < 8; e++) delta[e] = (c1*(-ph[e]) + c2*ht[e]) * iv;
+      }
+      float d0s = 0, d1s = 0, d2s = 0;
+#pragma unroll
+      for (int e = 0; e < 8; e++) {
+        const float ww = pz[e]*delta[e];
+        d0s += delta[e]*delta[e]; d1s += ww*ww; d2s += ph[e]*ww;
+      }
+      d0s = wave_sum(d0s); d1s = wave_sum(d1s); d2s = wave_sum(d2s);
+      const float dn = sqrtf(fmaxf(d0s, EPSF));
+      const float axnd = artanh_c(dn);
+      const float wxn = sqrtf(fmaxf(d1s, EPSF));
+      const float tzd = tanhf(wxn / dn * axnd);
+      const float szd = (wxn <= 1e-7f) ? 0.f : tzd/wxn;
+      const float y2zd = (wxn <= 1e-7f) ? 0.f : tzd*tzd;
+      {
+        const float xy = szd * d2s;
+        const float iv = 1.f / fmaxf(1.f + 2.f*xy + p_sh2*y2zd, EPSF);
+        const float c1 = 1.f + 2.f*xy + y2zd, c2 = 1.f - p_sh2;
+#pragma unroll
+        for (int q = 0; q < 2; q++) {
+          ushort th[4], tl[4]; float hv[4];
+#pragma unroll
+          for (int i = 0; i < 4; i++) {
+            const int e = q*4 + i;
+            hv[i] = (c1*ph[e] + c2*(szd*pz[e]*delta[e])) * iv;
+            split2(hv[i], th[i], tl[i]);
+          }
+          ((ushort4*)(A.Hh + (size_t)row*512))[lane + 64*q] = make_ushort4(th[0],th[1],th[2],th[3]);
+          ((ushort4*)(A.Hl + (size_t)row*512))[lane + 64*q] = make_ushort4(tl[0],tl[1],tl[2],tl[3]);
+          if (s == 99)
+            ((float4*)(A.hbuf + (size_t)row*512))[lane + 64*q] = make_float4(hv[0],hv[1],hv[2],hv[3]);
+        }
+      }
+      if (s + 1 < 100) {
+        const int tok = (g ? A.tgt_t : A.src_t)[b*100 + s + 1];
+        const float fac = A.tokf[(g*512 + b)*100 + s + 1].x;
+        const float4 ev = ((const float4*)(A.emb + (size_t)tok*256))[lane];
+        ushort th[4], tl[4];
+#pragma unroll
+        for (int i = 0; i < 4; i++) split2(fac * F4E(ev,i), th[i], tl[i]);
+        ((ushort4*)(A.Xh + (size_t)row*256))[lane] = make_ushort4(th[0],th[1],th[2],th[3]);
+        ((ushort4*)(A.Xl + (size_t)row*256))[lane] = make_ushort4(tl[0],tl[1],tl[2],tl[3]);
+      }
+    }
+    grid.sync();
+  }
+
+  if (bid < 32) {
+    const int erow = (bid >> 3) * 128, ecol = (bid & 7) * 64;
+    const int mat = (bid & 7) >> 2;
+    const int colM = ((bid & 7) & 3) * 64;
+    const size_t Woff = (size_t)mat*131072 + (size_t)colM*512;
+    const int r_l0 = erow + wrA*32 + fr, r_l1 = r_l0 + 16;
+    const int arow0 = mat ? (512 + A.alignment[r_l0]) : r_l0;
+    const int arow1 = mat ? (512 + A.alignment[r_l1]) : r_l1;
+    const size_t a0 = (size_t)arow0*512 + kg*8, a1 = (size_t)arow1*512 + kg*8;
+    const size_t b0 = (size_t)(wcA*32 + fr)*512 + kg*8, b1 = b0 + (size_t)16*512;
+    float* outB = A.mxb + (size_t)(erow + wrA*32)*512 + (ecol + wcA*32 + fr);
+    mma_32x32(A.Hh, A.Hl, a0, a1, A.W2h + Woff, A.W2l + Woff, b0, b1, 512, outB, 512, kg);
+  }
+  grid.sync();
+
+  if (w < 2) {
+    const int fb = bid*2 + w;
+    const int ar = 512 + A.alignment[fb];
+    float hs[8], htg[8];
+    float a0 = 0, a1 = 0, a2 = 0;
+#pragma unroll
+    for (int q = 0; q < 2; q++) {
+      const int j4 = lane + 64*q;
+      const float4 v1 = ((const float4*)(A.hbuf + (size_t)fb*512))[j4];
+      const float4 v2 = ((const float4*)(A.hbuf + (size_t)ar*512))[j4];
+#pragma unroll
+      for (int i = 0; i < 4; i++) {
+        const int e = q*4 + i;
+        hs[e] = F4E(v1,i); htg[e] = F4E(v2,i);
+        a0 += hs[e]*hs[e]; a1 += htg[e]*htg[e]; a2 += hs[e]*htg[e];
+      }
+    }
+    float mxs[4], mxt[4], bps[4], bpt[4], db[4], pp0[4], pp1[4], pa0[4], pa1[4];
+    {
+      const float4 vm0 = ((const float4*)(A.mxb + (size_t)fb*512))[lane];
+      const float4 vm1 = ((const float4*)(A.mxb + (size_t)fb*512 + 256))[lane];
+      const float4 vbs = ((const float4*)A.bp_src)[lane];
+      const float4 vbt = ((const float4*)A.bp_tgt)[lane];
+      const float4 vdb = ((const float4*)A.dist_bias)[lane];
+      const float4 vp0 = ((const float4*)A.plane_p)[lane];
+      const float4 vp1 = ((const float4*)(A.plane_p + 256))[lane];
+      const float4 va0 = ((const float4*)A.plane_a)[lane];
+      const float4 va1 = ((const float4*)(A.plane_a + 256))[lane];
+#pragma unroll
+      for (int i = 0; i < 4; i++) {
+        mxs[i] = F4E(vm0,i); mxt[i] = F4E(vm1,i);
+        bps[i] = F4E(vbs,i); bpt[i] = F4E(vbt,i); db[i] = F4E(vdb,i);
+        pp0[i] = F4E(vp0,i); pp1[i] = F4E(vp1,i);
+        pa0[i] = F4E(va0,i); pa1[i] = F4E(va1,i);
+      }
+    }
+    float a3 = 0, a4 = 0;
+#pragma unroll
+    for (int i = 0; i < 4; i++) { a3 += mxs[i]*mxs[i]; a4 += mxt[i]*mxt[i]; }
+    a0 = wave_sum(a0); a1 = wave_sum(a1); a2 = wave_sum(a2);
+    a3 = wave_sum(a3); a4 = wave_sum(a4);
+    const float shs = a0, sht = a1, dot_st = a2;
+    const float xns = sqrtf(fmaxf(shs, EPSF)), axns = artanh_c(xns);
+    const float xnt = sqrtf(fmaxf(sht, EPSF)), axnt = artanh_c(xnt);
+    const float ms = sqrtf(fmaxf(a3, EPSF)); const float ts = tanhf(ms / xns * axns);
+    const float ss = (ms <= 1e-7f) ? 0.f : ts/ms; const float x2s = (ms <= 1e-7f) ? 0.f : ts*ts;
+    const float mt = sqrtf(fmaxf(a4, EPSF)); const float tt = tanhf(mt / xnt * axnt);
+    const float st = (mt <= 1e-7f) ? 0.f : tt/mt; const float x2t = (mt <= 1e-7f) ? 0.f : tt*tt;
+    float vs[4], vt[4];
+#pragma unroll
+    for (int i = 0; i < 4; i++) { vs[i] = ss*mxs[i]; vt[i] = st*mxt[i]; }
+    float rb0=0, rb1=0, rb2=0, rb3=0, rb4=0;
+#pragma unroll
+    for (int i = 0; i < 4; i++) {
+      rb0 += bps[i]*bps[i]; rb1 += vs[i]*bps[i];
+      rb2 += bpt[i]*bpt[i]; rb3 += vt[i]*bpt[i]; rb4 += db[i]*db[i];
+    }
+    rb0 = wave_sum(rb0); rb1 = wave_sum(rb1); rb2 = wave_sum(rb2);
+    rb3 = wave_sum(rb3); rb4 = wave_sum(rb4);
+    float ps[4], pt[4];
+    {
+      const float iv = 1.f / fmaxf(1.f + 2.f*rb1 + x2s*rb0, EPSF);
+      const float c1 = 1.f + 2.f*rb1 + rb0, c2 = 1.f - x2s;
+#pragma unroll
+      for (int i = 0; i < 4; i++) ps[i] = (c1*vs[i] + c2*bps[i]) * iv;
+    }
+    {
+      const float iv = 1.f / fmaxf(1.f + 2.f*rb3 + x2t*rb2, EPSF);
+      const float c1 = 1.f + 2.f*rb3 + rb2, c2 = 1.f - x2t;
+#pragma unroll
+      for (int i = 0; i < 4; i++) pt[i] = (c1*vt[i] + c2*bpt[i]) * iv;
+    }
+    float rc0 = 0, rc1 = 0;
+#pragma unroll
+    for (int i = 0; i < 4; i++) { rc0 += ps[i]*ps[i]; rc1 += pt[i]*pt[i]; }
+    rc0 = wave_sum(rc0); rc1 = wave_sum(rc1);
+    {
+      const float n = sqrtf(fmaxf(rc0, EPSF));
+      if (n > 0.999f) { const float sc = 0.999f/n;
+#pragma unroll
+        for (int i = 0; i < 4; i++) ps[i] *= sc; }
+    }
+    {
+      const float n = sqrtf(fmaxf(rc1, EPSF));
+      if (n > 0.999f) { const float sc = 0.999f/n;
+#pragma unroll
+        for (int i = 0; i < 4; i++) pt[i] *= sc; }
+    }
+    float df2 = 0;
+    {
+      const float xy = -dot_st;
+      const float iv = 1.f / fmaxf(1.f + 2.f*xy + shs*sht, EPSF);
+      const float c1 = 1.f + 2.f*xy + sht, c2 = 1.f - shs;
+#pragma unroll
+      for (int e = 0; e < 8; e++) { const float d = (c1*(-hs[e]) + c2*htg[e]) * iv; df2 += d*d; }
+    }
+    float rd0=0, rd1=0, rd2=0;
+#pragma unroll
+    for (int i = 0; i < 4; i++) { rd0 += ps[i]*ps[i]; rd1 += pt[i]*pt[i]; rd2 += ps[i]*pt[i]; }
+    rd0 = wave_sum(rd0); rd1 = wave_sum(rd1); rd2 = wave_sum(rd2);
+    const float rd3 = wave_sum(df2);
+    float pr[4];
+    {
+      const float iv = 1.f / fmaxf(1.f + 2.f*rd2 + rd0*rd1, EPSF);
+      const float c1 = 1.f + 2.f*rd2 + rd1, c2 = 1.f - rd0;
+#pragma unroll
+      for (int i = 0; i < 4; i++) pr[i] = (c1*ps[i] + c2*pt[i]) * iv;
+    }
+    const float dn = sqrtf(fmaxf(rd3, EPSF));
+    const float dist = 2.f * artanh_c(dn);
+    const float d2v = dist * dist;
+    const float dbn = sqrtf(fmaxf(rb4, EPSF));
+    const float bscale = tanhf(d2v * artanh_c(dbn)) / dbn;
+    float biasv[4];
+#pragma unroll
+    for (int i = 0; i < 4; i++) biasv[i] = bscale * db[i];
+    float re0=0, re1=0, re2=0;
+#pragma unroll
+    for (int i = 0; i < 4; i++) { re0 += pr[i]*pr[i]; re1 += biasv[i]*biasv[i]; re2 += pr[i]*biasv[i]; }
+    re0 = wave_sum(re0); re1 = wave_sum(re1); re2 = wave_sum(re2);
+    float pr2[4];
+    {
+      const float iv = 1.f / fmaxf(1.f + 2.f*re2 + re0*re1, EPSF);
+      const float c1 = 1.f + 2.f*re2 + re1, c2 = 1.f - re0;
+#pragma unroll
+      for (int i = 0; i < 4; i++) pr2[i] = (c1*pr[i] + c2*biasv[i]) * iv;
+    }
+    float rf0=0, rf1=0, rf2=0, rf3=0, rf4=0;
+#pragma unroll
+    for (int i = 0; i < 4; i++) {
+      rf0 += pp0[i]*pp0[i]; rf1 += pp0[i]*pr2[i];
+      rf2 += pp1[i]*pp1[i]; rf3 += pp1[i]*pr2[i]; rf4 += pr2[i]*pr2[i];
+    }
+    rf0 = wave_sum(rf0); rf1 = wave_sum(rf1); rf2 = wave_sum(rf2);
+    rf3 = wave_sum(rf3); rf4 = wave_sum(rf4);
+    float d0v[4], d1v[4];
+    {
+      const float xy = -rf1;
+      const float iv = 1.f / fmaxf(1.f + 2.f*xy + rf0*rf4, EPSF);
+      const float c1 = 1.f + 2.f*xy + rf4, c2 = 1.f - rf0;
+#pragma unroll
+      for (int i = 0; i < 4; i++) d0v[i] = (c1*(-pp0[i]) + c2*pr2[i]) * iv;
+    }
+    {
+      const float xy = -rf3;
+      const float iv = 1.f / fmaxf(1.f + 2.f*xy + rf2*rf4, EPSF);
+      const float c1 = 1.f + 2.f*xy + rf4, c2 = 1.f - rf2;
+#pragma unroll
+      for (int i = 0; i < 4; i++) d1v[i] = (c1*(-pp1[i]) + c2*pr2[i]) * iv;
+    }
+    float rg0=0, rg1=0, rg2=0, rg3=0, rg4=0, rg5=0;
+#pragma unroll
+    for (int i = 0; i < 4; i++) {
+      rg0 += d0v[i]*d0v[i]; rg1 += d0v[i]*pa0[i]; rg2 += pa0[i]*pa0[i];
+      rg3 += d1v[i]*d1v[i]; rg4 += d1v[i]*pa1[i]; rg5 += pa1[i]*pa1[i];
+    }
+    rg0 = wave_sum(rg0); rg1 = wave_sum(rg1); rg2 = wave_sum(rg2);
+    rg3 = wave_sum(rg3); rg4 = wave_sum(rg4); rg5 = wave_sum(rg5);
+    if (lane == 0) {
+      const float an0 = sqrtf(fmaxf(rg2, EPSF));
+      const float an1 = sqrtf(fmaxf(rg5, EPSF));
+      A.outp[fb*2 + 0] = asinhf(2.f * rg1 / fmaxf((1.f - rg0) * an0, EPSF));
+      A.outp[fb*2 + 1] = asinhf(2.f * rg4 / fmaxf((1.f - rg3) * an1, EPSF));
+    }
   }
 }
 
@@ -500,32 +684,41 @@
   const int* alignment   = (const int*)d_in[16];
   float* outp            = (float*)d_out;
 
-  float* ws = (float*)d_ws;
-  float* hbuf = ws + 0;
-  float* xbuf = ws + 524288;
-  float* g1   = ws + 786432;
-  float* zb   = ws + 3407872;
-  float* rhb  = ws + 3932160;
-  float* uhxb = ws + 4456448;
-  float* htm  = ws + 4980736;
-  float* rn   = ws + 5505024;
-  float4* tokf = (float4*)(ws + 5513216);
-  float* mxb  = ws + 5922816;
-
-  hipMemsetAsync(hbuf, 0, 1024 * 512 * sizeof(float), stream);
+  char* wsb = (char*)d_ws;
+  float*  g1   = (float*)(wsb + 0);
+  float*  htm  = (float*)(wsb + 10485760);
+  float*  hbuf = (float*)(wsb + 12582912);
+  float*  mxb  = (float*)(wsb + 14680064);
+  float4* tokf = (float4*)(wsb + 15728640);
+  bf16*   Hh   = (bf16*)(wsb + 17367040);
+  bf16*   Hl   = (bf16*)(wsb + 18415616);
+  bf16*   Xh   = (bf16*)(wsb + 19464192);
+  bf16*   Xl   = (bf16*)(wsb + 19988480);
+  bf16*   Rh   = (bf16*)(wsb + 20512768);
+  bf16*   Rl   = (bf16*)(wsb + 21561344);
+  bf16*   W0h  = (bf16*)(wsb + 22609920);
+  bf16*   W0l  = (bf16*)(wsb + 26279936);
+  bf16*   W1h  = (bf16*)(wsb + 29949952);
+  bf16*   W1l  = (bf16*)(wsb + 30998528);
+  bf16*   W2h  = (bf16*)(wsb + 32047104);
+  bf16*   W2l  = (bf16*)(wsb + 32571392);
+
+  hipMemsetAsync(Hh, 0, 1048576, stream);
+  hipMemsetAsync(Hl, 0, 1048576, stream);
+  k_wconv<<<10240, 256, 0, stream>>>(w_ih_src, w_hh_src, w_ih_tgt, w_hh_tgt,
+                                     wp_src, wp_tgt, W0h, W0l, W1h, W1l, W2h, W2l);
   k_tok<<<25600, 256, 0, stream>>>(emb, src_t, tgt_t, tokf);
-  kx0<<<1024, 256, 0, stream>>>(emb, src_t, tgt_t, tokf, xbuf);
-  for (int s = 0; s < 100; s++) {
-    gemm_k<<<dim3(16, 40), 256, 0, stream>>>(0, hbuf, xbuf, rhb,
-        w_ih_src, w_hh_src, w_ih_tgt, w_hh_tgt, wp_src, wp_tgt, alignment, g1);
-    k2_gates<<<1024, 256, 0, stream>>>(g1, hbuf, b_src, b_tgt, tokf, zb, rhb, uhxb, rn, s);
-    gemm_k<<<dim3(16, 8), 256, 0, stream>>>(1, hbuf, xbuf, rhb,
-        w_ih_src, w_hh_src, w_ih_tgt, w_hh_tgt, wp_src, wp_tgt, alignment, htm);
-    k4_update<<<1024, 256, 0, stream>>>(htm, uhxb, zb, hbuf, b_src, b_tgt, rn, tokf,
-        src_t, tgt_t, emb, xbuf, s);
-  }
-  gemm_k<<<dim3(8, 8), 256, 0, stream>>>(2, hbuf, xbuf, rhb,
-      w_ih_src, w_hh_src, w_ih_tgt, w_hh_tgt, wp_src, wp_tgt, alignment, mxb);
-  k_head<<<512, 256, 0, stream>>>(hbuf, mxb, bp_src, bp_tgt, dist_bias,
-      plane_p, plane_a, alignment, outp);
-}
+  kx0<<<1024, 256, 0, stream>>>(emb, src_t, tgt_t, tokf, Xh, Xl);
+
+  CoopArgs A;
+  A.emb = emb; A.src_t = src_t; A.tgt_t = tgt_t;
+  A.b_src = b_src; A.b_tgt = b_tgt; A.bp_src = bp_src; A.bp_tgt = bp_tgt;
+  A.dist_bias = dist_bias; A.plane_p = plane_p; A.plane_a = plane_a;
+  A.alignment = alignment;
+  A.g1 = g1; A.htm = htm; A.hbuf = hbuf; A.mxb = mxb; A.tokf = tokf;
+  A.Hh = Hh; A.Hl = Hl; A.Xh = Xh; A.Xl = Xl; A.Rh = Rh; A.Rl = Rl;
+  A.W0h = W0h; A.W0l = W0l; A.W1h = W1h; A.W1l = W1l; A.W2h = W2h; A.W2l = W2l;
+  A.outp = outp;
+  void* kargs[] = { &A };
+  hipLaunchCooperativeKernel((void*)k_coop, dim3(256), dim3(512), kargs, 0, stream);
+}
```

After: 18.63 ms. 132% more time.
